# Performance work log

Measured on AMD Instinct MI355X. Metric: run time of the kernel, lower is better.

The kernel has to match this reference:

```python
import jax, jax.numpy as jnp
import numpy as np

B, BEAM, TMAX, V, D, H, NL, S, DFF = 4, 5, 16, 50257, 768, 12, 2, 128, 3072
BUF = TMAX + 1  # prefix buffer: sos + TMAX generated tokens
DH = D // H
SOS, EOS = 1, 2
NEG = -1e20


def _ln(x, g, b):
    m = x.mean(-1, keepdims=True)
    v = ((x - m) ** 2).mean(-1, keepdims=True)
    return (x - m) / jnp.sqrt(v + 1e-5) * g + b


def _mha(q_in, kv_in, in_w, in_b, out_w, out_b, bias=None, kpm=None):
    # PyTorch-style MHA: packed in_proj [3D, D], out_proj [D, D]
    q = q_in @ in_w[:D].T + in_b[:D]
    k = kv_in @ in_w[D:2 * D].T + in_b[D:2 * D]
    v = kv_in @ in_w[2 * D:].T + in_b[2 * D:]
    Bq, Tq = q.shape[0], q.shape[1]
    Tk = k.shape[1]
    q = q.reshape(Bq, Tq, H, DH)
    k = k.reshape(Bq, Tk, H, DH)
    v = v.reshape(Bq, Tk, H, DH)
    s = jnp.einsum('bqhd,bkhd->bhqk', q, k) * (1.0 / np.sqrt(DH))
    if bias is not None:
        s = s + bias  # additive causal bias (-10000 * (1 - tril)), as in source
    if kpm is not None:
        s = jnp.where(kpm[:, None, None, :], -1e9, s)  # memory_key_padding_mask
    a = jax.nn.softmax(s, axis=-1)
    o = jnp.einsum('bhqk,bkhd->bqhd', a, v).reshape(Bq, Tq, D)
    return o @ out_w.T + out_b


def _decode(emb, pos, ln_emb_g, ln_emb_b, self_in_w, self_in_b, self_out_w,
            self_out_b, cross_in_w, cross_in_b, cross_out_w, cross_out_b,
            ff1_w, ff1_b, ff2_w, ff2_b, ln1_g, ln1_b, ln2_g, ln2_b, ln3_g,
            ln3_b, dense_w, dense_b, context, source_mask):
    causal = -10000.0 * (1.0 - jnp.tril(jnp.ones((BUF, BUF), jnp.float32)))
    mem = jnp.repeat(context, BEAM, axis=0)            # [B*BEAM, S, D]
    kpm = jnp.repeat(source_mask == 0, BEAM, axis=0)   # True = pad
    # Beam init: nextYs[0] = [sos, 0, 0, ...]; scores trick makes step-0 pick
    # from beam row 0 only, matching beamLk = wordLk[0] in the source.
    buf0 = jnp.zeros((B, BEAM, BUF), jnp.int32).at[:, 0, 0].set(SOS)
    s0 = jnp.concatenate([jnp.zeros((1,), jnp.float32),
                          jnp.full((BEAM - 1,), NEG, jnp.float32)])
    scores0 = jnp.broadcast_to(s0, (B, BEAM))

    def step(carry, t):
        scores, buf = carry
        # no KV cache: re-run full decoder each step (fixed-size padded buffer;
        # causal mask makes positions <= t identical to running on the prefix)
        x = emb[buf.reshape(B * BEAM, BUF)] + pos[None, :BUF]
        x = _ln(x, ln_emb_g, ln_emb_b)
        for l in range(NL):  # post-norm TransformerDecoderLayer, dropout=eval
            sa = _mha(x, x, self_in_w[l], self_in_b[l], self_out_w[l],
                      self_out_b[l], bias=causal)
            x = _ln(x + sa, ln1_g[l], ln1_b[l])
            ca = _mha(x, mem, cross_in_w[l], cross_in_b[l], cross_out_w[l],
                      cross_out_b[l], kpm=kpm)
            x = _ln(x + ca, ln2_g[l], ln2_b[l])
            ff = jax.nn.relu(x @ ff1_w[l].T + ff1_b[l]) @ ff2_w[l].T + ff2_b[l]
            x = _ln(x + ff, ln3_g[l], ln3_b[l])
        h = jnp.tanh(jnp.take(x, t, axis=1) @ dense_w.T + dense_b)  # last pos
        logp = jax.nn.log_softmax(h @ emb.T, axis=-1).reshape(B, BEAM, V)
        last = jnp.take(buf, t, axis=2)  # previous token per beam
        beamLk = logp + scores[:, :, None]
        beamLk = jnp.where((last == EOS)[:, :, None], NEG, beamLk)
        vals, ids = jax.lax.top_k(beamLk.reshape(B, BEAM * V), BEAM)
        prevK = ids // V
        tok = (ids % V).astype(jnp.int32)
        buf = jnp.take_along_axis(buf, prevK[:, :, None], axis=1)
        buf = buf.at[:, :, t + 1].set(tok)
        return (vals, buf), None

    (scores, buf), _ = jax.lax.scan(step, (scores0, buf0), jnp.arange(TMAX))
    toks = buf[:, :, 1:]                         # backtracked hypotheses
    keep = jnp.cumsum(toks == EOS, axis=-1) == 0  # truncate at eos, pad with 0
    preds = jnp.where(keep, toks, 0)
    return scores, preds


def setup_inputs() -> dict:
    key = jax.random.key(0)
    ks = jax.random.split(key, 12)
    r = lambda k, shape: jax.random.normal(k, shape, jnp.float32) * 0.02
    inp = {}
    inp['emb'] = r(ks[0], (V, D))
    inp['pos'] = r(ks[1], (BUF, D))
    inp['ln_emb_g'] = jnp.ones((D,), jnp.float32)
    inp['ln_emb_b'] = jnp.zeros((D,), jnp.float32)
    inp['self_in_w'] = r(ks[2], (NL, 3 * D, D))
    inp['self_in_b'] = jnp.zeros((NL, 3 * D), jnp.float32)
    inp['self_out_w'] = r(ks[3], (NL, D, D))
    inp['self_out_b'] = jnp.zeros((NL, D), jnp.float32)
    inp['cross_in_w'] = r(ks[4], (NL, 3 * D, D))
    inp['cross_in_b'] = jnp.zeros((NL, 3 * D), jnp.float32)
    inp['cross_out_w'] = r(ks[5], (NL, D, D))
    inp['cross_out_b'] = jnp.zeros((NL, D), jnp.float32)
    inp['ff1_w'] = r(ks[6], (NL, DFF, D))
    inp['ff1_b'] = jnp.zeros((NL, DFF), jnp.float32)
    inp['ff2_w'] = r(ks[7], (NL, D, DFF))
    inp['ff2_b'] = jnp.zeros((NL, D), jnp.float32)
    inp['ln1_g'] = jnp.ones((NL, D), jnp.float32)
    inp['ln1_b'] = jnp.zeros((NL, D), jnp.float32)
    inp['ln2_g'] = jnp.ones((NL, D), jnp.float32)
    inp['ln2_b'] = jnp.zeros((NL, D), jnp.float32)
    inp['ln3_g'] = jnp.ones((NL, D), jnp.float32)
    inp['ln3_b'] = jnp.zeros((NL, D), jnp.float32)
    inp['dense_w'] = r(ks[8], (D, D))
    inp['dense_b'] = jnp.zeros((D,), jnp.float32)
    inp['context'] = jax.random.normal(ks[9], (B, S, D), jnp.float32)
    inp['source_mask'] = jnp.ones((B, S), jnp.int32)
    return inp


def reference(emb, pos, ln_emb_g, ln_emb_b, self_in_w, self_in_b, self_out_w,
              self_out_b, cross_in_w, cross_in_b, cross_out_w, cross_out_b,
              ff1_w, ff1_b, ff2_w, ff2_b, ln1_g, ln1_b, ln2_g, ln2_b, ln3_g,
              ln3_b, dense_w, dense_b, context, source_mask):
    return _decode(emb, pos, ln_emb_g, ln_emb_b, self_in_w, self_in_b,
                   self_out_w, self_out_b, cross_in_w, cross_in_b,
                   cross_out_w, cross_out_b, ff1_w, ff1_b, ff2_w, ff2_b,
                   ln1_g, ln1_b, ln2_g, ln2_b, ln3_g, ln3_b, dense_w,
                   dense_b, context, source_mask)
```

## Files before the change

### kernel.cpp

```cpp
#include <hip/hip_runtime.h>
#include <cfloat>
#include <cmath>

constexpr int kV   = 50257;
constexpr int kVP  = 50432;
constexpr int kD   = 768;
constexpr int NLY  = 2;
constexpr int BB   = 4;
constexpr int BEAM = 5;
constexpr int RR   = BB * BEAM;
constexpr int BUFL = 17;
constexpr int SS   = 128;
constexpr int DFF  = 3072;
constexpr int TMAX = 16;
constexpr int SOS  = 1;
constexpr int EOSt = 2;
constexpr int LB   = (kV + 255) / 256;
#define NEGV (-1e20f)

__device__ inline float wave_sum(float v) {
#pragma unroll
  for (int o = 32; o > 0; o >>= 1) v += __shfl_xor(v, o, 64);
  return v;
}
__device__ inline float wave_max(float v) {
#pragma unroll
  for (int o = 32; o > 0; o >>= 1) v = fmaxf(v, __shfl_xor(v, o, 64));
  return v;
}
__device__ inline bool better(float v1, int i1, float v2, int i2) {
  return v1 > v2 || (v1 == v2 && i1 < i2);
}
__device__ inline void insert5(float* tv, int* ti, float v, int i) {
  if (better(v, i, tv[4], ti[4])) {
    tv[4] = v; ti[4] = i;
#pragma unroll
    for (int s = 4; s > 0; --s)
      if (better(tv[s], ti[s], tv[s - 1], ti[s - 1])) {
        float fv = tv[s]; tv[s] = tv[s - 1]; tv[s - 1] = fv;
        int iv = ti[s]; ti[s] = ti[s - 1]; ti[s - 1] = iv;
      }
  }
}
__device__ inline float sel5f(const float* a, int i) {
  float r = a[0];
  r = (i == 1) ? a[1] : r; r = (i == 2) ? a[2] : r;
  r = (i == 3) ? a[3] : r; r = (i == 4) ? a[4] : r;
  return r;
}
__device__ inline int sel5i(const int* a, int i) {
  int r = a[0];
  r = (i == 1) ? a[1] : r; r = (i == 2) ? a[2] : r;
  r = (i == 3) ? a[3] : r; r = (i == 4) ? a[4] : r;
  return r;
}
__device__ inline void merge5(float* av, int* ai, const float* bv, const int* bi) {
  float cv[5]; int ci[5];
  int ia = 0, ib = 0;
#pragma unroll
  for (int s = 0; s < 5; ++s) {
    float va = sel5f(av, ia); int xa = sel5i(ai, ia);
    float vb = sel5f(bv, ib); int xb = sel5i(bi, ib);
    bool ta = better(va, xa, vb, xb);
    cv[s] = ta ? va : vb; ci[s] = ta ? xa : xb;
    ia += ta ? 1 : 0; ib += ta ? 0 : 1;
  }
#pragma unroll
  for (int s = 0; s < 5; ++s) { av[s] = cv[s]; ai[s] = ci[s]; }
}

__global__ void init_k(int* buf0, float* scores) {
  int tid = threadIdx.x;
  if (tid < RR * BUFL) buf0[tid] = 0;
  __syncthreads();
  if (tid < BB) buf0[tid * BEAM * BUFL] = SOS;
  if (tid < RR) scores[tid] = (tid % BEAM == 0) ? 0.f : NEGV;
}

__global__ void transpose_k(const float* __restrict__ src, float* __restrict__ dst,
                            int R, int C, int ds) {
  __shared__ float tile[32][33];
  const int c0 = blockIdx.x * 32, r0 = blockIdx.y * 32;
  const int lx = threadIdx.x & 31, ly = threadIdx.x >> 5;
#pragma unroll
  for (int j = 0; j < 4; ++j) {
    int r = r0 + ly + j * 8;
    if (r < R && c0 + lx < C) tile[ly + j * 8][lx] = src[(size_t)r * C + c0 + lx];
  }
  __syncthreads();
#pragma unroll
  for (int j = 0; j < 4; ++j) {
    int c = c0 + ly + j * 8;
    if (c < C && r0 + lx < R) dst[(size_t)c * ds + r0 + lx] = tile[lx][ly + j * 8];
  }
}

template<bool WT>
__global__ __launch_bounds__(256) void crosskv_k(
    const float* __restrict__ ctx, const float* __restrict__ Wm0,
    const float* __restrict__ bias0, float* __restrict__ ck, float* __restrict__ cv) {
  const int l = blockIdx.z;
  const float* Wm = Wm0 + (size_t)l * 2304 * 768;
  const float* bias = bias0 + l * 2304;
  __shared__ float a_s[16 * 768];
  __shared__ float ps[4 * 64 * 17];
  const int tid = threadIdx.x;
  const int row0 = blockIdx.y * 16;
  for (int i = tid * 4; i < 16 * 768; i += 1024) {
    int rr = i / 768, k = i - rr * 768;
    *(float4*)&a_s[i] = *(const float4*)&ctx[(size_t)(row0 + rr) * 768 + k];
  }
  __syncthreads();
  const int w = tid >> 6, lane = tid & 63;
  const int colg = 768 + blockIdx.x * 64 + lane;
  const int kb = w * 192;
  float acc[16];
#pragma unroll
  for (int r = 0; r < 16; ++r) acc[r] = 0.f;
  for (int k4 = 0; k4 < 48; ++k4) {
    const int k = kb + k4 * 4;
    float w0, w1, w2, w3;
    if (WT) {
      w0 = Wm[(size_t)(k + 0) * 2304 + colg]; w1 = Wm[(size_t)(k + 1) * 2304 + colg];
      w2 = Wm[(size_t)(k + 2) * 2304 + colg]; w3 = Wm[(size_t)(k + 3) * 2304 + colg];
    } else {
      float4 wv = *(const float4*)&Wm[(size_t)colg * 768 + k];
      w0 = wv.x; w1 = wv.y; w2 = wv.z; w3 = wv.w;
    }
#pragma unroll
    for (int r = 0; r < 16; ++r) {
      float4 a = *(const float4*)&a_s[r * 768 + k];
      acc[r] = fmaf(a.x, w0, fmaf(a.y, w1, fmaf(a.z, w2, fmaf(a.w, w3, acc[r]))));
    }
  }
#pragma unroll
  for (int r = 0; r < 16; ++r) ps[(w * 64 + lane) * 17 + r] = acc[r];
  __syncthreads();
  for (int o = tid; o < 1024; o += 256) {
    int rr = o >> 6, cl = o & 63;
    int cg = 768 + blockIdx.x * 64 + cl;
    float v = bias[cg];
#pragma unroll
    for (int ww = 0; ww < 4; ++ww) v += ps[(ww * 64 + cl) * 17 + rr];
    int gr = row0 + rr;
    int b = gr >> 7, s = gr & 127;
    int c = cg - 768, kv = c / 768, n = c - kv * 768;
    float* dst = kv ? cv : ck;
    dst[((size_t)(l * 4 + b) * 128 + s) * 768 + n] = v;
  }
}

template<bool WT>
__global__ __launch_bounds__(256) void gemm20_k(
    const float* __restrict__ Wm, int wstride, const float* __restrict__ bias, int N,
    int pre, const float* __restrict__ xsrc, const float* __restrict__ tmp_in,
    const float* __restrict__ lng, const float* __restrict__ lnb, float* __restrict__ xout,
    int outmode, float* __restrict__ out0,
    float* __restrict__ kcl, float* __restrict__ vcl, int t,
    const float* __restrict__ embp, const float* __restrict__ posw, const int* __restrict__ bufn,
    int reorder_t, const float* __restrict__ kco, const float* __restrict__ vco,
    float* __restrict__ kcn, float* __restrict__ vcn, const int* __restrict__ prevK) {
  __shared__ float a_s[RR * 768];
  __shared__ float ps[4 * 64 * 21];
  __shared__ float mS[RR], rS[RR];
  __shared__ int tokS[RR];
  const int tid = threadIdx.x;

  if (reorder_t > 0) {
    const int per = 768 * reorder_t;
    const int tot = 2 * RR * per;
    for (int i = blockIdx.x * 256 + tid; i < tot; i += gridDim.x * 256) {
      int half = i / (RR * per);
      int rem = i - half * RR * per;
      int r = rem / per;
      int rem2 = rem - r * per;
      int p = rem2 / 768;
      int d = rem2 - p * 768;
      int src = (r / BEAM) * BEAM + prevK[r];
      if (half == 0) kcn[(r * BUFL + p) * 768 + d] = kco[(src * BUFL + p) * 768 + d];
      else           vcn[(r * BUFL + p) * 768 + d] = vco[(src * BUFL + p) * 768 + d];
    }
  }
  if (pre == 1 && tid < RR) tokS[tid] = bufn[tid * BUFL + t];
  __syncthreads();
  for (int i = tid * 4; i < RR * 768; i += 1024) {
    int r = i / 768, k = i - r * 768;
    float4 v;
    if (pre == 0) v = *(const float4*)&xsrc[i];
    else if (pre == 1) {
      float4 e = *(const float4*)&embp[(size_t)tokS[r] * 768 + k];
      float4 p = *(const float4*)&posw[(size_t)t * 768 + k];
      v = make_float4(e.x + p.x, e.y + p.y, e.z + p.z, e.w + p.w);
    } else {
      float4 a = *(const float4*)&xsrc[i];
      float4 b = *(const float4*)&tmp_in[i];
      v = make_float4(a.x + b.x, a.y + b.y, a.z + b.z, a.w + b.w);
    }
    *(float4*)&a_s[i] = v;
  }
  __syncthreads();
  if (pre != 0) {
    const int w0 = tid >> 6, ln = tid & 63;
    for (int r = w0 * 5; r < w0 * 5 + 5; ++r) {
      float s = 0.f, q = 0.f;
      for (int k = ln; k < 768; k += 64) { float v = a_s[r * 768 + k]; s += v; q += v * v; }
      s = wave_sum(s); q = wave_sum(q);
      if (ln == 0) {
        float m = s / 768.f;
        float var = q / 768.f - m * m;
        mS[r] = m; rS[r] = 1.f / sqrtf(var + 1e-5f);
      }
    }
    __syncthreads();
    for (int i = tid * 4; i < RR * 768; i += 1024) {
      int r = i / 768, k = i - r * 768;
      float4 v = *(const float4*)&a_s[i];
      float4 g = *(const float4*)&lng[k];
      float4 b = *(const float4*)&lnb[k];
      float m = mS[r], rs = rS[r];
      v = make_float4((v.x - m) * rs * g.x + b.x, (v.y - m) * rs * g.y + b.y,
                      (v.z - m) * rs * g.z + b.z, (v.w - m) * rs * g.w + b.w);
      *(float4*)&a_s[i] = v;
    }
    __syncthreads();
    if (xout != nullptr && blockIdx.x == 0) {
      for (int i = tid * 4; i < RR * 768; i += 1024)
        *(float4*)&xout[i] = *(const float4*)&a_s[i];
    }
  }
  const int w = tid >> 6, lane = tid & 63;
  const int colg = blockIdx.x * 64 + lane;
  const int kb = w * 192;
  float acc[RR];
#pragma unroll
  for (int r = 0; r < RR; ++r) acc[r] = 0.f;
  for (int k4 = 0; k4 < 48; ++k4) {
    const int k = kb + k4 * 4;
    float w0, w1, w2, w3;
    if (WT) {
      w0 = Wm[(size_t)(k + 0) * wstride + colg]; w1 = Wm[(size_t)(k + 1) * wstride + colg];
      w2 = Wm[(size_t)(k + 2) * wstride + colg]; w3 = Wm[(size_t)(k + 3) * wstride + colg];
    } else {
      float4 wv = *(const float4*)&Wm[(size_t)colg * 768 + k];
      w0 = wv.x; w1 = wv.y; w2 = wv.z; w3 = wv.w;
    }
#pragma unroll
    for (int r = 0; r < RR; ++r) {
      float4 a = *(const float4*)&a_s[r * 768 + k];
      acc[r] = fmaf(a.x, w0, fmaf(a.y, w1, fmaf(a.z, w2, fmaf(a.w, w3, acc[r]))));
    }
  }
#pragma unroll
  for (int r = 0; r < RR; ++r) ps[(w * 64 + lane) * 21 + r] = acc[r];
  __syncthreads();
  for (int o = tid; o < RR * 64; o += 256) {
    int r = o >> 6, cl = o & 63;
    int cg = blockIdx.x * 64 + cl;
    float v = bias[cg];
#pragma unroll
    for (int ww = 0; ww < 4; ++ww) v += ps[(ww * 64 + cl) * 21 + r];
    if (outmode == 1) v = fmaxf(v, 0.f);
    else if (outmode == 2) v = tanhf(v);
    if (outmode == 3) {
      if (cg < 768) out0[r * 768 + cg];
      if (cg < 768) out0[r * 768 + cg] = v;
      else if (cg < 1536) kcl[(r * BUFL + t) * 768 + (cg - 768)] = v;
      else vcl[(r * BUFL + t) * 768 + (cg - 1536)] = v;
    } else {
      out0[(size_t)r * N + cg] = v;
    }
  }
}

template<bool WT>
__global__ __launch_bounds__(1024) void ff2_k(
    const float* __restrict__ Wm, const float* __restrict__ bias,
    const float* __restrict__ A, float* __restrict__ out0) {
  __shared__ float ps[64 * 16 * 21];
  const int tid = threadIdx.x;
  const int w = tid >> 6, lane = tid & 63;
  const int cl = lane & 15, ksub = lane >> 4;
  const int colg = blockIdx.x * 16 + cl;
  const int kb = w * 192 + ksub * 48;
  float acc[RR];
#pragma unroll
  for (int r = 0; r < RR; ++r) acc[r] = 0.f;
  for (int k4 = 0; k4 < 12; ++k4) {
    const int k = kb + k4 * 4;
    float w0, w1, w2, w3;
    if (WT) {
      w0 = Wm[(size_t)(k + 0) * 768 + colg]; w1 = Wm[(size_t)(k + 1) * 768 + colg];
      w2 = Wm[(size_t)(k + 2) * 768 + colg]; w3 = Wm[(size_t)(k + 3) * 768 + colg];
    } else {
      float4 wv = *(const float4*)&Wm[(size_t)colg * 3072 + k];
      w0 = wv.x; w1 = wv.y; w2 = wv.z; w3 = wv.w;
    }
#pragma unroll
    for (int r = 0; r < RR; ++r) {
      float4 a = *(const float4*)&A[r * 3072 + k];
      acc[r] = fmaf(a.x, w0, fmaf(a.y, w1, fmaf(a.z, w2, fmaf(a.w, w3, acc[r]))));
    }
  }
  const int seg = w * 4 + ksub;
#pragma unroll
  for (int r = 0; r < RR; ++r) ps[(seg * 16 + cl) * 21 + r] = acc[r];
  __syncthreads();
  if (tid < RR * 16) {
    int r = tid >> 4, c2 = tid & 15;
    float v = bias[blockIdx.x * 16 + c2];
    for (int s2 = 0; s2 < 64; ++s2) v += ps[(s2 * 16 + c2) * 21 + r];
    out0[r * 768 + blockIdx.x * 16 + c2] = v;
  }
}

__global__ __launch_bounds__(64) void self_attn_k(
    const float* __restrict__ qb, const float* __restrict__ kcn,
    const float* __restrict__ vcn, float* __restrict__ outb, int t) {
  const int r = blockIdx.x, hh = blockIdx.y, lane = threadIdx.x;
  __shared__ float qs[64];
  __shared__ float ks[16 * 65];
  __shared__ float pp[16];
  qs[lane] = qb[r * 768 + hh * 64 + lane];
  for (int p = 0; p <= t; ++p)
    ks[p * 65 + lane] = kcn[(r * BUFL + p) * 768 + hh * 64 + lane];
  __syncthreads();
  float s = -1e30f;
  if (lane <= t) {
    float a = 0.f;
#pragma unroll
    for (int d = 0; d < 64; ++d) a = fmaf(qs[d], ks[lane * 65 + d], a);
    s = a * 0.125f;
  }
  float m = wave_max(s);
  float p = expf(s - m);
  float sum = wave_sum(p);
  if (lane <= t) pp[lane] = p / sum;
  __syncthreads();
  const float* vb = vcn + r * BUFL * 768 + hh * 64 + lane;
  float o = 0.f;
  for (int k = 0; k <= t; ++k) o = fmaf(pp[k], vb[k * 768], o);
  outb[r * 768 + hh * 64 + lane] = o;
}

__global__ __launch_bounds__(64) void cross_attn_k(
    const float* __restrict__ qb, const float* __restrict__ ck,
    const float* __restrict__ cv, const int* __restrict__ smask,
    float* __restrict__ outb) {
  const int r = blockIdx.x, hh = blockIdx.y, lane = threadIdx.x;
  const int b = r / BEAM;
  __shared__ float qs[64];
  __shared__ float ks[128 * 65];
  __shared__ float pp[128];
  qs[lane] = qb[r * 768 + hh * 64 + lane];
  for (int p = 0; p < 128; ++p)
    ks[p * 65 + lane] = ck[((size_t)b * 128 + p) * 768 + hh * 64 + lane];
  __syncthreads();
  float a0 = 0.f, a1 = 0.f;
#pragma unroll
  for (int d = 0; d < 64; ++d) {
    a0 = fmaf(qs[d], ks[lane * 65 + d], a0);
    a1 = fmaf(qs[d], ks[(lane + 64) * 65 + d], a1);
  }
  float s0 = a0 * 0.125f, s1 = a1 * 0.125f;
  if (smask[b * 128 + lane] == 0)      s0 = -1e9f;
  if (smask[b * 128 + lane + 64] == 0) s1 = -1e9f;
  float m = wave_max(fmaxf(s0, s1));
  float p0 = expf(s0 - m), p1 = expf(s1 - m);
  float sum = wave_sum(p0 + p1);
  pp[lane] = p0 / sum; pp[lane + 64] = p1 / sum;
  __syncthreads();
  const float* vb = cv + (size_t)b * 128 * 768 + hh * 64 + lane;
  float o0 = 0.f, o1 = 0.f, o2 = 0.f, o3 = 0.f;
  for (int k = 0; k < 128; k += 4) {
    o0 = fmaf(pp[k + 0], vb[(k + 0) * 768], o0);
    o1 = fmaf(pp[k + 1], vb[(k + 1) * 768], o1);
    o2 = fmaf(pp[k + 2], vb[(k + 2) * 768], o2);
    o3 = fmaf(pp[k + 3], vb[(k + 3) * 768], o3);
  }
  outb[r * 768 + hh * 64 + lane] = (o0 + o1) + (o2 + o3);
}

template<bool ET>
__global__ __launch_bounds__(256) void logits_k(
    const float* __restrict__ hbuf, const float* __restrict__ embM,
    float* __restrict__ candV, int* __restrict__ candI,
    float* __restrict__ mrow, float* __restrict__ srow) {
  __shared__ float hs[RR * 768];
  __shared__ float vv[4 * 256];
  const int tid = threadIdx.x, blk = blockIdx.x;
  for (int i = tid * 4; i < RR * 768; i += 1024)
    *(float4*)&hs[i] = *(const float4*)&hbuf[i];
  __syncthreads();
  const int col = blk * 256 + tid;
  const bool valid = col < kV;
  const int colc = valid ? col : (kV - 1);
  float acc[RR];
#pragma unroll
  for (int r = 0; r < RR; ++r) acc[r] = 0.f;
  for (int k = 0; k < 768; k += 4) {
    float w0, w1, w2, w3;
    if (ET) {
      w0 = embM[(size_t)(k + 0) * kVP + col]; w1 = embM[(size_t)(k + 1) * kVP + col];
      w2 = embM[(size_t)(k + 2) * kVP + col]; w3 = embM[(size_t)(k + 3) * kVP + col];
    } else {
      float4 wv = *(const float4*)&embM[(size_t)colc * 768 + k];
      w0 = wv.x; w1 = wv.y; w2 = wv.z; w3 = wv.w;
    }
#pragma unroll
    for (int r = 0; r < RR; ++r) {
      float4 a = *(const float4*)&hs[r * 768 + k];
      acc[r] = fmaf(a.x, w0, fmaf(a.y, w1, fmaf(a.z, w2, fmaf(a.w, w3, acc[r]))));
    }
  }
  const int w = tid >> 6, lane = tid & 63;
  for (int g = 0; g < 5; ++g) {
#pragma unroll
    for (int j = 0; j < 4; ++j) vv[j * 256 + tid] = valid ? acc[g * 4 + j] : -FLT_MAX;
    __syncthreads();
    const int r = g * 4 + w;
    float v[4]; int gc[4]; bool used[4];
#pragma unroll
    for (int j = 0; j < 4; ++j) {
      v[j] = vv[w * 256 + lane * 4 + j];
      gc[j] = blk * 256 + lane * 4 + j;
      used[j] = false;
    }
    float tv[5]; int tg[5];
#pragma unroll
    for (int round = 0; round < 5; ++round) {
      float bv = -FLT_MAX; int bidx = 0x7fffffff; int bj = -1;
#pragma unroll
      for (int j = 0; j < 4; ++j) {
        bool c = (!used[j]) && better(v[j], gc[j], bv, bidx);
        bv = c ? v[j] : bv; bidx = c ? gc[j] : bidx; bj = c ? j : bj;
      }
      float wv2 = bv; int wi = bidx;
      for (int d = 1; d < 64; d <<= 1) {
        float ov = __shfl_xor(wv2, d, 64); int oi = __shfl_xor(wi, d, 64);
        if (better(ov, oi, wv2, wi)) { wv2 = ov; wi = oi; }
      }
      tv[round] = wv2; tg[round] = wi;
      if (bj >= 0 && bidx == wi) used[bj] = true;
    }
    float m = tv[0];
    float s = 0.f;
#pragma unroll
    for (int j = 0; j < 4; ++j) s += expf(v[j] - m);
    s = wave_sum(s);
    if (lane == 0) {
      mrow[r * LB + blk] = m;
      srow[r * LB + blk] = s;
#pragma unroll
      for (int q = 0; q < 5; ++q) {
        candV[(r * LB + blk) * 5 + q] = tv[q];
        candI[(r * LB + blk) * 5 + q] = tg[q];
      }
    }
    __syncthreads();
  }
}

__global__ __launch_bounds__(256) void topk_k(
    const float* __restrict__ candV, const int* __restrict__ candI,
    const float* __restrict__ mrow, const float* __restrict__ srow,
    float* __restrict__ scores, const int* __restrict__ bufc, int* __restrict__ bufn,
    int t, int* __restrict__ prevK, int* __restrict__ tokv) {
  const int b = blockIdx.x, tid = threadIdx.x;
  const int w = tid >> 6, lane = tid & 63;
  __shared__ float lseS[5], scS[5];
  __shared__ int emS[5];
  __shared__ float wv5[4][5]; __shared__ int wi5[4][5];
  __shared__ int fpk[5], ftok[5];
  for (int j = w; j < 5; j += 4) {
    const int gr = b * 5 + j;
    float M = -FLT_MAX, S = 0.f;
    for (int e = lane; e < LB; e += 64) {
      float m2 = mrow[gr * LB + e], s2 = srow[gr * LB + e];
      if (m2 > M) { S = S * expf(M - m2) + s2; M = m2; }
      else        { S += s2 * expf(m2 - M); }
    }
    for (int d = 1; d < 64; d <<= 1) {
      float Mo = __shfl_xor(M, d, 64), So = __shfl_xor(S, d, 64);
      float Mn = fmaxf(M, Mo);
      S = S * expf(M - Mn) + So * expf(Mo - Mn);
      M = Mn;
    }
    if (lane == 0) {
      lseS[j] = M + logf(S);
      scS[j] = scores[gr];
      emS[j] = (bufc[gr * BUFL + t] == EOSt);
    }
  }
  __syncthreads();
  float tv[5]; int ti[5];
#pragma unroll
  for (int s = 0; s < 5; ++s) { tv[s] = -FLT_MAX; ti[s] = 0x7fffffff; }
  for (int i = tid; i < 5 * LB * 5; i += 256) {
    int j = i / (LB * 5);
    int e = i - j * LB * 5;
    int blk = e / 5, rk = e - blk * 5;
    int gr = b * 5 + j;
    float cvv = candV[(gr * LB + blk) * 5 + rk];
    int col = candI[(gr * LB + blk) * 5 + rk];
    float val = emS[j] ? NEGV : (cvv - lseS[j] + scS[j]);
    insert5(tv, ti, val, j * kV + col);
  }
  for (int d = 1; d < 64; d <<= 1) {
    float ov[5]; int oi[5];
#pragma unroll
    for (int s = 0; s < 5; ++s) { ov[s] = __shfl_xor(tv[s], d, 64); oi[s] = __shfl_xor(ti[s], d, 64); }
    merge5(tv, ti, ov, oi);
  }
  if (lane == 0) {
#pragma unroll
    for (int s = 0; s < 5; ++s) { wv5[w][s] = tv[s]; wi5[w][s] = ti[s]; }
  }
  __syncthreads();
  if (tid == 0) {
    float av[5]; int ai[5];
#pragma unroll
    for (int s = 0; s < 5; ++s) { av[s] = wv5[0][s]; ai[s] = wi5[0][s]; }
    for (int ww = 1; ww < 4; ++ww) {
      float bv[5]; int bi[5];
#pragma unroll
      for (int s = 0; s < 5; ++s) { bv[s] = wv5[ww][s]; bi[s] = wi5[ww][s]; }
      merge5(av, ai, bv, bi);
    }
#pragma unroll
    for (int s = 0; s < 5; ++s) {
      int pk = ai[s] / kV;
      int tk = ai[s] - pk * kV;
      scores[b * 5 + s] = av[s];
      prevK[b * 5 + s] = pk; tokv[b * 5 + s] = tk;
      fpk[s] = pk; ftok[s] = tk;
    }
  }
  __syncthreads();
  for (int i = tid; i < 5 * BUFL; i += 256) {
    int j = i / BUFL, p = i - j * BUFL;
    int src = b * 5 + fpk[j];
    int val = (p == t + 1) ? ftok[j] : bufc[src * BUFL + p];
    bufn[(b * 5 + j) * BUFL + p] = val;
  }
}

__global__ void finalize_k(const float* __restrict__ scores, const int* __restrict__ buf,
                           float* __restrict__ out) {
  const int tid = threadIdx.x;
  if (tid < RR) {
    out[tid] = scores[tid];
    int seen = 0;
    for (int i = 0; i < TMAX; ++i) {
      int tk = buf[tid * BUFL + 1 + i];
      if (tk == EOSt) seen = 1;
      out[RR + tid * TMAX + i] = seen ? 0.f : (float)tk;
    }
  }
}

extern "C" void kernel_launch(void* const* d_in, const int* in_sizes, int n_in,
                              void* d_out, int out_size, void* d_ws, size_t ws_size,
                              hipStream_t stream) {
  const float* emb        = (const float*)d_in[0];
  const float* pos        = (const float*)d_in[1];
  const float* ln_emb_g   = (const float*)d_in[2];
  const float* ln_emb_b   = (const float*)d_in[3];
  const float* self_in_w  = (const float*)d_in[4];
  const float* self_in_b  = (const float*)d_in[5];
  const float* self_out_w = (const float*)d_in[6];
  const float* self_out_b = (const float*)d_in[7];
  const float* cross_in_w = (const float*)d_in[8];
  const float* cross_in_b = (const float*)d_in[9];
  const float* cross_out_w= (const float*)d_in[10];
  const float* cross_out_b= (const float*)d_in[11];
  const float* ff1_w      = (const float*)d_in[12];
  const float* ff1_b      = (const float*)d_in[13];
  const float* ff2_w      = (const float*)d_in[14];
  const float* ff2_b      = (const float*)d_in[15];
  const float* ln1_g      = (const float*)d_in[16];
  const float* ln1_b      = (const float*)d_in[17];
  const float* ln2_g      = (const float*)d_in[18];
  const float* ln2_b      = (const float*)d_in[19];
  const float* ln3_g      = (const float*)d_in[20];
  const float* ln3_b      = (const float*)d_in[21];
  const float* dense_w    = (const float*)d_in[22];
  const float* dense_b    = (const float*)d_in[23];
  const float* context    = (const float*)d_in[24];
  const int*   source_mask= (const int*)d_in[25];

  float* wsf = (float*)d_ws;
  size_t off = 0;
  auto alloc = [&](size_t n) { float* p = wsf + off; off += (n + 3) & ~(size_t)3; return p; };

  float* XA    = alloc(RR * 768);
  float* XB    = alloc(RR * 768);
  float* XC    = alloc(RR * 768);
  float* qb    = alloc(RR * 768);
  float* attnb = alloc(RR * 768);
  float* tmp   = alloc(RR * 768);
  float* hbuf  = alloc(RR * 768);
  float* ffb   = alloc(RR * 3072);
  float* candV = alloc(RR * LB * 5);
  float* mrow  = alloc(RR * LB);
  float* srow  = alloc(RR * LB);
  float* scores= alloc(32);
  float* ck    = alloc((size_t)NLY * 4 * 128 * 768);
  float* cv    = alloc((size_t)NLY * 4 * 128 * 768);
  const size_t cacheSeg = (size_t)RR * BUFL * 768;
  float* kcB   = alloc(4 * cacheSeg);
  float* vcB   = alloc(4 * cacheSeg);
  int* candI   = (int*)alloc(RR * LB * 5);
  int* bufs0   = (int*)alloc(RR * BUFL + 12);
  int* bufs1   = (int*)alloc(RR * BUFL + 12);
  int* prevKp  = (int*)alloc(32);
  int* tokp    = (int*)alloc(32);
  const size_t baseFloats = off;

  const size_t nSiT = (size_t)768 * 2304, nSoT = (size_t)768 * 768;
  const size_t nCiT = nSiT, nCoT = nSoT, nF1T = (size_t)768 * 3072, nF2T = (size_t)3072 * 768;
  const size_t wtFloats = 2 * (nSiT + nSoT + nCiT + nCoT + nF1T + nF2T) + nSoT;
  const size_t embTFloats = (size_t)768 * kVP;
  const bool useWT = ws_size >= (baseFloats + wtFloats) * 4;
  const bool useET = useWT && ws_size >= (baseFloats + wtFloats + embTFloats) * 4;

  float* siT[2]; float* soT[2]; float* ciT[2]; float* coT[2]; float* f1T[2]; float* f2T[2];
  float* dT = nullptr; float* embT = nullptr;
  if (useWT) {
    for (int l = 0; l < 2; ++l) siT[l] = alloc(nSiT);
    for (int l = 0; l < 2; ++l) soT[l] = alloc(nSoT);
    for (int l = 0; l < 2; ++l) ciT[l] = alloc(nCiT);
    for (int l = 0; l < 2; ++l) coT[l] = alloc(nCoT);
    for (int l = 0; l < 2; ++l) f1T[l] = alloc(nF1T);
    for (int l = 0; l < 2; ++l) f2T[l] = alloc(nF2T);
    dT = alloc(nSoT);
    if (useET) embT = alloc(embTFloats);
  }

  init_k<<<1, 512, 0, stream>>>(bufs0, scores);

  if (useWT) {
    auto T = [&](const float* src, float* dst, int R, int C, int ds) {
      dim3 g((C + 31) / 32, (R + 31) / 32);
      transpose_k<<<g, 256, 0, stream>>>(src, dst, R, C, ds);
    };
    for (int l = 0; l < 2; ++l) {
      T(self_in_w  + (size_t)l * 2304 * 768, siT[l], 2304, 768, 2304);
      T(self_out_w + (size_t)l * 768 * 768,  soT[l], 768, 768, 768);
      T(cross_in_w + (size_t)l * 2304 * 768, ciT[l], 2304, 768, 2304);
      T(cross_out_w+ (size_t)l * 768 * 768,  coT[l], 768, 768, 768);
      T(ff1_w      + (size_t)l * 3072 * 768, f1T[l], 3072, 768, 3072);
      T(ff2_w      + (size_t)l * 768 * 3072, f2T[l], 768, 3072, 768);
    }
    T(dense_w, dT, 768, 768, 768);
    if (useET) T(emb, embT, kV, 768, kVP);
  }

  {
    dim3 g(24, 32, 2);
    if (useWT) crosskv_k<true><<<g, 256, 0, stream>>>(context, ciT[0], cross_in_b, ck, cv);
    else       crosskv_k<false><<<g, 256, 0, stream>>>(context, cross_in_w, cross_in_b, ck, cv);
  }

  const int* bc = bufs0;
  auto G = [&](const float* Wt, const float* Wg, int wstride,
               const float* bias, int N, int pre, const float* xsrc, const float* tmpin,
               const float* g2, const float* b2, float* xout, int outmode, float* out0,
               float* kcl, float* vcl, int tt,
               int reorder_t, const float* kco, const float* vco, float* kcn2, float* vcn2) {
    dim3 grid(N / 64);
    if (useWT)
      gemm20_k<true><<<grid, 256, 0, stream>>>(Wt, wstride, bias, N, pre, xsrc, tmpin, g2, b2,
        xout, outmode, out0, kcl, vcl, tt, emb, pos, bc, reorder_t, kco, vco, kcn2, vcn2, prevKp);
    else
      gemm20_k<false><<<grid, 256, 0, stream>>>(Wg, wstride, bias, N, pre, xsrc, tmpin, g2, b2,
        xout, outmode, out0, kcl, vcl, tt, emb, pos, bc, reorder_t, kco, vco, kcn2, vcn2, prevKp);
  };

  for (int t = 0; t < TMAX; ++t) {
    bc = (t & 1) ? bufs1 : bufs0;
    int* bn = (t & 1) ? bufs0 : bufs1;
    const int np = (t + 1) & 1, op = t & 1;

    for (int l = 0; l < 2; ++l) {
      float* kNew = kcB + (np * 2 + l) * cacheSeg;
      float* vNew = vcB + (np * 2 + l) * cacheSeg;
      float* kOld = kcB + (op * 2 + l) * cacheSeg;
      float* vOld = vcB + (op * 2 + l) * cacheSeg;
      if (l == 0)
        G(siT[0], self_in_w, 2304, self_in_b, 2304,
          1, nullptr, nullptr, ln_emb_g, ln_emb_b, XA,
          3, qb, kNew, vNew, t, t, kOld, vOld, kNew, vNew);
      else
        G(siT[1], self_in_w + (size_t)2304 * 768, 2304, self_in_b + 2304, 2304,
          2, XC, tmp, ln3_g, ln3_b, XA,
          3, qb, kNew, vNew, t, t, kOld, vOld, kNew, vNew);
      self_attn_k<<<dim3(RR, 12), 64, 0, stream>>>(qb, kNew, vNew, attnb, t);
      G(soT[l], self_out_w + (size_t)l * 768 * 768, 768, self_out_b + l * 768, 768,
        0, attnb, nullptr, nullptr, nullptr, nullptr, 0, tmp,
        nullptr, nullptr, t, 0, nullptr, nullptr, nullptr, nullptr);
      G(ciT[l], cross_in_w + (size_t)l * 2304 * 768, 2304, cross_in_b + l * 2304, 768,
        2, XA, tmp, ln1_g + l * 768, ln1_b + l * 768, XB, 0, qb,
        nullptr, nullptr, t, 0, nullptr, nullptr, nullptr, nullptr);
      cross_attn_k<<<dim3(RR, 12), 64, 0, stream>>>(
          qb, ck + (size_t)l * 4 * 128 * 768, cv + (size_t)l * 4 * 128 * 768, source_mask, attnb);
      G(coT[l], cross_out_w + (size_t)l * 768 * 768, 768, cross_out_b + l * 768, 768,
        0, attnb, nullptr, nullptr, nullptr, nullptr, 0, tmp,
        nullptr, nullptr, t, 0, nullptr, nullptr, nullptr, nullptr);
      G(f1T[l], ff1_w + (size_t)l * 3072 * 768, 3072, ff1_b + l * 3072, 3072,
        2, XB, tmp, ln2_g + l * 768, ln2_b + l * 768, XC, 1, ffb,
        nullptr, nullptr, t, 0, nullptr, nullptr, nullptr, nullptr);
      if (useWT) ff2_k<true><<<48, 1024, 0, stream>>>(f2T[l], ff2_b + l * 768, ffb, tmp);
      else       ff2_k<false><<<48, 1024, 0, stream>>>(ff2_w + (size_t)l * 768 * 3072, ff2_b + l * 768, ffb, tmp);
    }
    G(dT, dense_w, 768, dense_b, 768,
      2, XC, tmp, ln3_g + 768, ln3_b + 768, nullptr, 2, hbuf,
      nullptr, nullptr, t, 0, nullptr, nullptr, nullptr, nullptr);
    if (useET) logits_k<true><<<LB, 256, 0, stream>>>(hbuf, embT, candV, candI, mrow, srow);
    else       logits_k<false><<<LB, 256, 0, stream>>>(hbuf, emb, candV, candI, mrow, srow);
    topk_k<<<BB, 256, 0, stream>>>(candV, candI, mrow, srow, scores, bc, bn, t, prevKp, tokp);
  }

  finalize_k<<<1, 64, 0, stream>>>(scores, bufs0, (float*)d_out);
}
```

Before: 11.20 ms.

## Fuse whole beam-search decode into a persistent megakernel with grid barriers

```diff
diff --git a/kernel.cpp b/kernel.cpp
--- a/kernel.cpp
+++ b/kernel.cpp
@@ -4,34 +4,31 @@
 
 constexpr int kV   = 50257;
 constexpr int kVP  = 50432;
-constexpr int kD   = 768;
-constexpr int NLY  = 2;
 constexpr int BB   = 4;
 constexpr int BEAM = 5;
-constexpr int RR   = BB * BEAM;
+constexpr int RR   = 20;
 constexpr int BUFL = 17;
-constexpr int SS   = 128;
-constexpr int DFF  = 3072;
 constexpr int TMAX = 16;
 constexpr int SOS  = 1;
 constexpr int EOSt = 2;
 constexpr int LB   = (kV + 255) / 256;
+constexpr int CSEG = RR * BUFL * 768;
 #define NEGV (-1e20f)
 
-__device__ inline float wave_sum(float v) {
+__device__ __forceinline__ float wave_sum(float v) {
 #pragma unroll
   for (int o = 32; o > 0; o >>= 1) v += __shfl_xor(v, o, 64);
   return v;
 }
-__device__ inline float wave_max(float v) {
+__device__ __forceinline__ float wave_max(float v) {
 #pragma unroll
   for (int o = 32; o > 0; o >>= 1) v = fmaxf(v, __shfl_xor(v, o, 64));
   return v;
 }
-__device__ inline bool better(float v1, int i1, float v2, int i2) {
+__device__ __forceinline__ bool better(float v1, int i1, float v2, int i2) {
   return v1 > v2 || (v1 == v2 && i1 < i2);
 }
-__device__ inline void insert5(float* tv, int* ti, float v, int i) {
+__device__ __forceinline__ void insert5(float* tv, int* ti, float v, int i) {
   if (better(v, i, tv[4], ti[4])) {
     tv[4] = v; ti[4] = i;
 #pragma unroll
@@ -42,19 +39,19 @@
       }
   }
 }
-__device__ inline float sel5f(const float* a, int i) {
+__device__ __forceinline__ float sel5f(const float* a, int i) {
   float r = a[0];
   r = (i == 1) ? a[1] : r; r = (i == 2) ? a[2] : r;
   r = (i == 3) ? a[3] : r; r = (i == 4) ? a[4] : r;
   return r;
 }
-__device__ inline int sel5i(const int* a, int i) {
+__device__ __forceinline__ int sel5i(const int* a, int i) {
   int r = a[0];
   r = (i == 1) ? a[1] : r; r = (i == 2) ? a[2] : r;
   r = (i == 3) ? a[3] : r; r = (i == 4) ? a[4] : r;
   return r;
 }
-__device__ inline void merge5(float* av, int* ai, const float* bv, const int* bi) {
+__device__ __forceinline__ void merge5(float* av, int* ai, const float* bv, const int* bi) {
   float cv[5]; int ci[5];
   int ia = 0, ib = 0;
 #pragma unroll
@@ -69,327 +66,340 @@
   for (int s = 0; s < 5; ++s) { av[s] = cv[s]; ai[s] = ci[s]; }
 }
 
-__global__ void init_k(int* buf0, float* scores) {
-  int tid = threadIdx.x;
-  if (tid < RR * BUFL) buf0[tid] = 0;
-  __syncthreads();
-  if (tid < BB) buf0[tid * BEAM * BUFL] = SOS;
-  if (tid < RR) scores[tid] = (tid % BEAM == 0) ? 0.f : NEGV;
-}
-
-__global__ void transpose_k(const float* __restrict__ src, float* __restrict__ dst,
-                            int R, int C, int ds) {
-  __shared__ float tile[32][33];
-  const int c0 = blockIdx.x * 32, r0 = blockIdx.y * 32;
-  const int lx = threadIdx.x & 31, ly = threadIdx.x >> 5;
-#pragma unroll
-  for (int j = 0; j < 4; ++j) {
-    int r = r0 + ly + j * 8;
-    if (r < R && c0 + lx < C) tile[ly + j * 8][lx] = src[(size_t)r * C + c0 + lx];
-  }
-  __syncthreads();
-#pragma unroll
-  for (int j = 0; j < 4; ++j) {
-    int c = c0 + ly + j * 8;
-    if (c < C && r0 + lx < R) dst[(size_t)c * ds + r0 + lx] = tile[lx][ly + j * 8];
+struct KParams {
+  const float *emb, *pos, *lneg, *lneb;
+  const float *siW, *siB, *soW, *soB, *ciW, *ciB, *coW, *coB;
+  const float *f1W, *f1B, *f2W, *f2B;
+  const float *ln1g, *ln1b, *ln2g, *ln2b, *ln3g, *ln3b;
+  const float *dW, *dB, *ctx;
+  const int* smask;
+  float *XA, *XB, *XC, *qb, *attnb, *tmp, *hbuf, *ffb;
+  float *fp0, *fp1, *fp2, *fp3;
+  float *candV, *mrow, *srow, *scores, *ck, *cv, *kcB, *vcB;
+  int *candI, *bufs0, *bufs1, *prevK, *tokv;
+  int *arrive, *release;
+  float *out;
+  float *siT, *soT, *ciT, *coT, *f1T, *f2T, *dT, *embT;
+  int useWT, useET;
+};
+
+__device__ __forceinline__ void gbar(int* arr, int* rel, int& ph) {
+  ++ph;
+  __syncthreads();
+  if (threadIdx.x == 0) {
+    __threadfence();
+    __hip_atomic_store(&arr[blockIdx.x], ph, __ATOMIC_RELAXED, __HIP_MEMORY_SCOPE_AGENT);
+  }
+  if (blockIdx.x == 0) {
+    while (__hip_atomic_load(&arr[threadIdx.x], __ATOMIC_RELAXED, __HIP_MEMORY_SCOPE_AGENT) < ph)
+      __builtin_amdgcn_s_sleep(2);
+    __syncthreads();
+    if (threadIdx.x == 0) {
+      __threadfence();
+      __hip_atomic_store(rel, ph, __ATOMIC_RELAXED, __HIP_MEMORY_SCOPE_AGENT);
+    }
+    __syncthreads();
+  } else {
+    if (threadIdx.x == 0) {
+      while (__hip_atomic_load(rel, __ATOMIC_RELAXED, __HIP_MEMORY_SCOPE_AGENT) < ph)
+        __builtin_amdgcn_s_sleep(2);
+      __threadfence();
+    }
+    __syncthreads();
+  }
+}
+
+__device__ void do_transposes(const KParams& P, float* SM) {
+  const float* srcs[14]; float* dsts[14]; int Rs[14], Cs[14], dss[14];
+  int nj = 0;
+  for (int l = 0; l < 2; ++l) { srcs[nj]=P.siW + (size_t)l*2304*768; dsts[nj]=P.siT + (size_t)l*768*2304; Rs[nj]=2304; Cs[nj]=768; dss[nj]=2304; ++nj; }
+  for (int l = 0; l < 2; ++l) { srcs[nj]=P.soW + (size_t)l*768*768;  dsts[nj]=P.soT + (size_t)l*768*768;  Rs[nj]=768;  Cs[nj]=768; dss[nj]=768;  ++nj; }
+  for (int l = 0; l < 2; ++l) { srcs[nj]=P.ciW + (size_t)l*2304*768; dsts[nj]=P.ciT + (size_t)l*768*2304; Rs[nj]=2304; Cs[nj]=768; dss[nj]=2304; ++nj; }
+  for (int l = 0; l < 2; ++l) { srcs[nj]=P.coW + (size_t)l*768*768;  dsts[nj]=P.coT + (size_t)l*768*768;  Rs[nj]=768;  Cs[nj]=768; dss[nj]=768;  ++nj; }
+  for (int l = 0; l < 2; ++l) { srcs[nj]=P.f1W + (size_t)l*3072*768; dsts[nj]=P.f1T + (size_t)l*768*3072; Rs[nj]=3072; Cs[nj]=768; dss[nj]=3072; ++nj; }
+  for (int l = 0; l < 2; ++l) { srcs[nj]=P.f2W + (size_t)l*768*3072; dsts[nj]=P.f2T + (size_t)l*3072*768; Rs[nj]=768;  Cs[nj]=3072; dss[nj]=768; ++nj; }
+  srcs[nj]=P.dW; dsts[nj]=P.dT; Rs[nj]=768; Cs[nj]=768; dss[nj]=768; ++nj;
+  if (P.useET) { srcs[nj]=P.emb; dsts[nj]=P.embT; Rs[nj]=kV; Cs[nj]=768; dss[nj]=kVP; ++nj; }
+  int tcnt[14], tot = 0;
+  for (int j = 0; j < nj; ++j) { tcnt[j] = ((Rs[j]+31)/32) * ((Cs[j]+31)/32); tot += tcnt[j]; }
+  const int tid = threadIdx.x;
+  const int lx = tid & 31, ly = tid >> 5;
+  for (int jt = blockIdx.x; jt < tot; jt += 256) {
+    int j = 0, lt = jt;
+    while (lt >= tcnt[j]) { lt -= tcnt[j]; ++j; }
+    int ct = (Cs[j] + 31) / 32;
+    int tr = lt / ct, tc = lt - tr * ct;
+    const float* src = srcs[j]; float* dst = dsts[j];
+    int R = Rs[j], C = Cs[j], ds = dss[j];
+    int r0 = tr * 32, c0 = tc * 32;
+    __syncthreads();
+#pragma unroll
+    for (int q = 0; q < 4; ++q) {
+      int r = r0 + ly + q * 8;
+      if (r < R && c0 + lx < C) SM[(ly + q * 8) * 33 + lx] = src[(size_t)r * C + c0 + lx];
+    }
+    __syncthreads();
+#pragma unroll
+    for (int q = 0; q < 4; ++q) {
+      int c = c0 + ly + q * 8;
+      if (c < C && r0 + lx < R) dst[(size_t)c * ds + r0 + lx] = SM[lx * 33 + ly + q * 8];
+    }
   }
 }
 
 template<bool WT>
-__global__ __launch_bounds__(256) void crosskv_k(
-    const float* __restrict__ ctx, const float* __restrict__ Wm0,
-    const float* __restrict__ bias0, float* __restrict__ ck, float* __restrict__ cv) {
-  const int l = blockIdx.z;
-  const float* Wm = Wm0 + (size_t)l * 2304 * 768;
-  const float* bias = bias0 + l * 2304;
-  __shared__ float a_s[16 * 768];
-  __shared__ float ps[4 * 64 * 17];
-  const int tid = threadIdx.x;
-  const int row0 = blockIdx.y * 16;
-  for (int i = tid * 4; i < 16 * 768; i += 1024) {
-    int rr = i / 768, k = i - rr * 768;
-    *(float4*)&a_s[i] = *(const float4*)&ctx[(size_t)(row0 + rr) * 768 + k];
-  }
-  __syncthreads();
-  const int w = tid >> 6, lane = tid & 63;
-  const int colg = 768 + blockIdx.x * 64 + lane;
-  const int kb = w * 192;
-  float acc[16];
-#pragma unroll
-  for (int r = 0; r < 16; ++r) acc[r] = 0.f;
-  for (int k4 = 0; k4 < 48; ++k4) {
-    const int k = kb + k4 * 4;
-    float w0, w1, w2, w3;
-    if (WT) {
-      w0 = Wm[(size_t)(k + 0) * 2304 + colg]; w1 = Wm[(size_t)(k + 1) * 2304 + colg];
-      w2 = Wm[(size_t)(k + 2) * 2304 + colg]; w3 = Wm[(size_t)(k + 3) * 2304 + colg];
-    } else {
-      float4 wv = *(const float4*)&Wm[(size_t)colg * 768 + k];
-      w0 = wv.x; w1 = wv.y; w2 = wv.z; w3 = wv.w;
-    }
-#pragma unroll
-    for (int r = 0; r < 16; ++r) {
-      float4 a = *(const float4*)&a_s[r * 768 + k];
-      acc[r] = fmaf(a.x, w0, fmaf(a.y, w1, fmaf(a.z, w2, fmaf(a.w, w3, acc[r]))));
-    }
-  }
-#pragma unroll
-  for (int r = 0; r < 16; ++r) ps[(w * 64 + lane) * 17 + r] = acc[r];
-  __syncthreads();
-  for (int o = tid; o < 1024; o += 256) {
-    int rr = o >> 6, cl = o & 63;
-    int cg = 768 + blockIdx.x * 64 + cl;
-    float v = bias[cg];
-#pragma unroll
-    for (int ww = 0; ww < 4; ++ww) v += ps[(ww * 64 + cl) * 17 + rr];
-    int gr = row0 + rr;
-    int b = gr >> 7, s = gr & 127;
-    int c = cg - 768, kv = c / 768, n = c - kv * 768;
-    float* dst = kv ? cv : ck;
-    dst[((size_t)(l * 4 + b) * 128 + s) * 768 + n] = v;
-  }
-}
-
-template<bool WT>
-__global__ __launch_bounds__(256) void gemm20_k(
-    const float* __restrict__ Wm, int wstride, const float* __restrict__ bias, int N,
-    int pre, const float* __restrict__ xsrc, const float* __restrict__ tmp_in,
-    const float* __restrict__ lng, const float* __restrict__ lnb, float* __restrict__ xout,
-    int outmode, float* __restrict__ out0,
-    float* __restrict__ kcl, float* __restrict__ vcl, int t,
-    const float* __restrict__ embp, const float* __restrict__ posw, const int* __restrict__ bufn,
-    int reorder_t, const float* __restrict__ kco, const float* __restrict__ vco,
-    float* __restrict__ kcn, float* __restrict__ vcn, const int* __restrict__ prevK) {
-  __shared__ float a_s[RR * 768];
-  __shared__ float ps[4 * 64 * 21];
-  __shared__ float mS[RR], rS[RR];
-  __shared__ int tokS[RR];
-  const int tid = threadIdx.x;
-
-  if (reorder_t > 0) {
-    const int per = 768 * reorder_t;
-    const int tot = 2 * RR * per;
-    for (int i = blockIdx.x * 256 + tid; i < tot; i += gridDim.x * 256) {
-      int half = i / (RR * per);
-      int rem = i - half * RR * per;
-      int r = rem / per;
-      int rem2 = rem - r * per;
-      int p = rem2 / 768;
-      int d = rem2 - p * 768;
-      int src = (r / BEAM) * BEAM + prevK[r];
-      if (half == 0) kcn[(r * BUFL + p) * 768 + d] = kco[(src * BUFL + p) * 768 + d];
-      else           vcn[(r * BUFL + p) * 768 + d] = vco[(src * BUFL + p) * 768 + d];
-    }
-  }
-  if (pre == 1 && tid < RR) tokS[tid] = bufn[tid * BUFL + t];
-  __syncthreads();
-  for (int i = tid * 4; i < RR * 768; i += 1024) {
-    int r = i / 768, k = i - r * 768;
-    float4 v;
-    if (pre == 0) v = *(const float4*)&xsrc[i];
-    else if (pre == 1) {
-      float4 e = *(const float4*)&embp[(size_t)tokS[r] * 768 + k];
-      float4 p = *(const float4*)&posw[(size_t)t * 768 + k];
-      v = make_float4(e.x + p.x, e.y + p.y, e.z + p.z, e.w + p.w);
-    } else {
-      float4 a = *(const float4*)&xsrc[i];
-      float4 b = *(const float4*)&tmp_in[i];
-      v = make_float4(a.x + b.x, a.y + b.y, a.z + b.z, a.w + b.w);
-    }
-    *(float4*)&a_s[i] = v;
-  }
-  __syncthreads();
-  if (pre != 0) {
-    const int w0 = tid >> 6, ln = tid & 63;
-    for (int r = w0 * 5; r < w0 * 5 + 5; ++r) {
-      float s = 0.f, q = 0.f;
-      for (int k = ln; k < 768; k += 64) { float v = a_s[r * 768 + k]; s += v; q += v * v; }
-      s = wave_sum(s); q = wave_sum(q);
-      if (ln == 0) {
-        float m = s / 768.f;
-        float var = q / 768.f - m * m;
-        mS[r] = m; rS[r] = 1.f / sqrtf(var + 1e-5f);
-      }
-    }
-    __syncthreads();
-    for (int i = tid * 4; i < RR * 768; i += 1024) {
-      int r = i / 768, k = i - r * 768;
-      float4 v = *(const float4*)&a_s[i];
-      float4 g = *(const float4*)&lng[k];
-      float4 b = *(const float4*)&lnb[k];
-      float m = mS[r], rs = rS[r];
-      v = make_float4((v.x - m) * rs * g.x + b.x, (v.y - m) * rs * g.y + b.y,
-                      (v.z - m) * rs * g.z + b.z, (v.w - m) * rs * g.w + b.w);
-      *(float4*)&a_s[i] = v;
-    }
-    __syncthreads();
-    if (xout != nullptr && blockIdx.x == 0) {
-      for (int i = tid * 4; i < RR * 768; i += 1024)
-        *(float4*)&xout[i] = *(const float4*)&a_s[i];
-    }
-  }
-  const int w = tid >> 6, lane = tid & 63;
-  const int colg = blockIdx.x * 64 + lane;
-  const int kb = w * 192;
-  float acc[RR];
-#pragma unroll
-  for (int r = 0; r < RR; ++r) acc[r] = 0.f;
-  for (int k4 = 0; k4 < 48; ++k4) {
-    const int k = kb + k4 * 4;
-    float w0, w1, w2, w3;
-    if (WT) {
-      w0 = Wm[(size_t)(k + 0) * wstride + colg]; w1 = Wm[(size_t)(k + 1) * wstride + colg];
-      w2 = Wm[(size_t)(k + 2) * wstride + colg]; w3 = Wm[(size_t)(k + 3) * wstride + colg];
-    } else {
-      float4 wv = *(const float4*)&Wm[(size_t)colg * 768 + k];
-      w0 = wv.x; w1 = wv.y; w2 = wv.z; w3 = wv.w;
-    }
-#pragma unroll
-    for (int r = 0; r < RR; ++r) {
-      float4 a = *(const float4*)&a_s[r * 768 + k];
-      acc[r] = fmaf(a.x, w0, fmaf(a.y, w1, fmaf(a.z, w2, fmaf(a.w, w3, acc[r]))));
-    }
-  }
-#pragma unroll
-  for (int r = 0; r < RR; ++r) ps[(w * 64 + lane) * 21 + r] = acc[r];
-  __syncthreads();
-  for (int o = tid; o < RR * 64; o += 256) {
-    int r = o >> 6, cl = o & 63;
-    int cg = blockIdx.x * 64 + cl;
-    float v = bias[cg];
-#pragma unroll
-    for (int ww = 0; ww < 4; ++ww) v += ps[(ww * 64 + cl) * 21 + r];
-    if (outmode == 1) v = fmaxf(v, 0.f);
-    else if (outmode == 2) v = tanhf(v);
-    if (outmode == 3) {
-      if (cg < 768) out0[r * 768 + cg];
-      if (cg < 768) out0[r * 768 + cg] = v;
-      else if (cg < 1536) kcl[(r * BUFL + t) * 768 + (cg - 768)] = v;
-      else vcl[(r * BUFL + t) * 768 + (cg - 1536)] = v;
-    } else {
-      out0[(size_t)r * N + cg] = v;
-    }
-  }
-}
-
-template<bool WT>
-__global__ __launch_bounds__(1024) void ff2_k(
-    const float* __restrict__ Wm, const float* __restrict__ bias,
-    const float* __restrict__ A, float* __restrict__ out0) {
-  __shared__ float ps[64 * 16 * 21];
+__device__ void do_crosskv(const KParams& P, float* SM) {
+  float* a_s = SM;
+  float* ps  = SM + 12288;
   const int tid = threadIdx.x;
   const int w = tid >> 6, lane = tid & 63;
-  const int cl = lane & 15, ksub = lane >> 4;
-  const int colg = blockIdx.x * 16 + cl;
-  const int kb = w * 192 + ksub * 48;
-  float acc[RR];
-#pragma unroll
-  for (int r = 0; r < RR; ++r) acc[r] = 0.f;
-  for (int k4 = 0; k4 < 12; ++k4) {
-    const int k = kb + k4 * 4;
-    float w0, w1, w2, w3;
-    if (WT) {
-      w0 = Wm[(size_t)(k + 0) * 768 + colg]; w1 = Wm[(size_t)(k + 1) * 768 + colg];
-      w2 = Wm[(size_t)(k + 2) * 768 + colg]; w3 = Wm[(size_t)(k + 3) * 768 + colg];
-    } else {
-      float4 wv = *(const float4*)&Wm[(size_t)colg * 3072 + k];
-      w0 = wv.x; w1 = wv.y; w2 = wv.z; w3 = wv.w;
-    }
-#pragma unroll
-    for (int r = 0; r < RR; ++r) {
-      float4 a = *(const float4*)&A[r * 3072 + k];
-      acc[r] = fmaf(a.x, w0, fmaf(a.y, w1, fmaf(a.z, w2, fmaf(a.w, w3, acc[r]))));
-    }
-  }
-  const int seg = w * 4 + ksub;
-#pragma unroll
-  for (int r = 0; r < RR; ++r) ps[(seg * 16 + cl) * 21 + r] = acc[r];
-  __syncthreads();
-  if (tid < RR * 16) {
-    int r = tid >> 4, c2 = tid & 15;
-    float v = bias[blockIdx.x * 16 + c2];
-    for (int s2 = 0; s2 < 64; ++s2) v += ps[(s2 * 16 + c2) * 21 + r];
-    out0[r * 768 + blockIdx.x * 16 + c2] = v;
-  }
-}
-
-__global__ __launch_bounds__(64) void self_attn_k(
-    const float* __restrict__ qb, const float* __restrict__ kcn,
-    const float* __restrict__ vcn, float* __restrict__ outb, int t) {
-  const int r = blockIdx.x, hh = blockIdx.y, lane = threadIdx.x;
-  __shared__ float qs[64];
-  __shared__ float ks[16 * 65];
-  __shared__ float pp[16];
-  qs[lane] = qb[r * 768 + hh * 64 + lane];
-  for (int p = 0; p <= t; ++p)
-    ks[p * 65 + lane] = kcn[(r * BUFL + p) * 768 + hh * 64 + lane];
+  for (int i5 = 0; i5 < 6; ++i5) {
+    int j = blockIdx.x + 256 * i5;
+    int cx = j % 24, ry = (j / 24) % 32, l = j / 768;
+    const float* Wt = P.ciT + (size_t)l * 768 * 2304;
+    const float* Wg = P.ciW + (size_t)l * 2304 * 768;
+    const float* bias = P.ciB + l * 2304;
+    const int row0 = ry * 16;
+    __syncthreads();
+    for (int i = tid * 4; i < 16 * 768; i += 1024) {
+      int rr = i / 768, k = i - rr * 768;
+      *(float4*)&a_s[i] = *(const float4*)&P.ctx[(size_t)(row0 + rr) * 768 + k];
+    }
+    __syncthreads();
+    const int colg = 768 + cx * 64 + lane;
+    const int kb = w * 192;
+    float acc[16];
+#pragma unroll
+    for (int r = 0; r < 16; ++r) acc[r] = 0.f;
+    for (int k4 = 0; k4 < 48; ++k4) {
+      const int k = kb + k4 * 4;
+      float w0, w1, w2, w3;
+      if (WT) {
+        const float* wr = Wt + (size_t)k * 2304 + colg;
+        w0 = wr[0]; w1 = wr[2304]; w2 = wr[2 * 2304]; w3 = wr[3 * 2304];
+      } else {
+        float4 wv = *(const float4*)&Wg[(size_t)colg * 768 + k];
+        w0 = wv.x; w1 = wv.y; w2 = wv.z; w3 = wv.w;
+      }
+#pragma unroll
+      for (int r = 0; r < 16; ++r) {
+        float4 a = *(const float4*)&a_s[r * 768 + k];
+        acc[r] = fmaf(a.x, w0, fmaf(a.y, w1, fmaf(a.z, w2, fmaf(a.w, w3, acc[r]))));
+      }
+    }
+#pragma unroll
+    for (int r = 0; r < 16; ++r) ps[(w * 64 + lane) * 16 + r] = acc[r];
+    __syncthreads();
+    for (int o = tid; o < 1024; o += 256) {
+      int rr = o >> 6, cl = o & 63;
+      int cg = 768 + cx * 64 + cl;
+      float v = bias[cg];
+#pragma unroll
+      for (int ww = 0; ww < 4; ++ww) v += ps[(ww * 64 + cl) * 16 + rr];
+      int gr = row0 + rr;
+      int b = gr >> 7, s = gr & 127;
+      int c = cg - 768, kv = c / 768, n = c - kv * 768;
+      float* dst = kv ? P.cv : P.ck;
+      dst[((size_t)(l * 4 + b) * 128 + s) * 768 + n] = v;
+    }
+  }
+}
+
+template<bool WT>
+__device__ void gemm_tile(
+    float* SM, int tile,
+    const float* Wt, int wstride, const float* Wg, int wgK, int wRowOff,
+    const float* bias, bool addBias,
+    int pre, const float* aBase, int aStride,
+    const float* xsrc, const float* const* parts, int nparts,
+    const float* lng, const float* lnb, float* xout,
+    int outmode, float* out0, int Nout,
+    float* kNew, float* vNew, int t, const int* bufc,
+    const float* embw, const float* posw)
+{
+  float* a_s = SM;
+  float* ps  = SM + 7680;
+  float* mS  = SM + 12800;
+  float* rS  = SM + 12820;
+  int* tokS  = (int*)(SM + 12840);
+  const int tid = threadIdx.x;
+  const int w = tid >> 6, lane = tid & 63;
+  if (pre == 1 && tid < RR) tokS[tid] = bufc[tid * BUFL + t];
+  __syncthreads();
+  for (int rp = 0; rp < 2; ++rp) {
+    const int r0 = rp * 10;
+    for (int i = tid * 4; i < 7680; i += 1024) {
+      int rl = i / 768, k = i - rl * 768, r = r0 + rl;
+      float4 v;
+      if (pre == 0) v = *(const float4*)&aBase[(size_t)r * aStride + k];
+      else if (pre == 1) {
+        float4 e = *(const float4*)&embw[(size_t)tokS[r] * 768 + k];
+        float4 p = *(const float4*)&posw[(size_t)t * 768 + k];
+        v = make_float4(e.x + p.x, e.y + p.y, e.z + p.z, e.w + p.w);
+      } else {
+        v = *(const float4*)&xsrc[r * 768 + k];
+        for (int q = 0; q < nparts; ++q) {
+          float4 u = *(const float4*)&parts[q][r * 768 + k];
+          v.x += u.x; v.y += u.y; v.z += u.z; v.w += u.w;
+        }
+      }
+      *(float4*)&a_s[i] = v;
+    }
+    __syncthreads();
+    if (pre != 0) {
+      for (int rl = w; rl < 10; rl += 4) {
+        float s = 0.f, q = 0.f;
+        for (int k = lane; k < 768; k += 64) { float v = a_s[rl * 768 + k]; s += v; q += v * v; }
+        s = wave_sum(s); q = wave_sum(q);
+        if (lane == 0) {
+          float m = s / 768.f;
+          mS[rl] = m; rS[rl] = 1.f / sqrtf(q / 768.f - m * m + 1e-5f);
+        }
+      }
+      __syncthreads();
+      for (int i = tid * 4; i < 7680; i += 1024) {
+        int rl = i / 768, k = i - rl * 768;
+        float4 v = *(const float4*)&a_s[i];
+        float4 g = *(const float4*)&lng[k];
+        float4 b = *(const float4*)&lnb[k];
+        float m = mS[rl], rs = rS[rl];
+        v = make_float4((v.x - m) * rs * g.x + b.x, (v.y - m) * rs * g.y + b.y,
+                        (v.z - m) * rs * g.z + b.z, (v.w - m) * rs * g.w + b.w);
+        *(float4*)&a_s[i] = v;
+        if (xout != nullptr && tile == 0) *(float4*)&xout[(r0 + rl) * 768 + k] = v;
+      }
+      __syncthreads();
+    }
+    const int c0 = tile * 128 + lane;
+    const int kb = w * 192;
+    float acc0[10], acc1[10];
+#pragma unroll
+    for (int rl = 0; rl < 10; ++rl) { acc0[rl] = 0.f; acc1[rl] = 0.f; }
+    for (int k4 = 0; k4 < 48; ++k4) {
+      const int k = kb + k4 * 4, kg = wRowOff + k;
+      float wa0, wa1, wa2, wa3, wb0, wb1, wb2, wb3;
+      if (WT) {
+        const float* wr = Wt + (size_t)kg * wstride;
+        wa0 = wr[c0]; wb0 = wr[c0 + 64]; wr += wstride;
+        wa1 = wr[c0]; wb1 = wr[c0 + 64]; wr += wstride;
+        wa2 = wr[c0]; wb2 = wr[c0 + 64]; wr += wstride;
+        wa3 = wr[c0]; wb3 = wr[c0 + 64];
+      } else {
+        float4 A4 = *(const float4*)&Wg[(size_t)c0 * wgK + kg];
+        float4 B4 = *(const float4*)&Wg[(size_t)(c0 + 64) * wgK + kg];
+        wa0 = A4.x; wa1 = A4.y; wa2 = A4.z; wa3 = A4.w;
+        wb0 = B4.x; wb1 = B4.y; wb2 = B4.z; wb3 = B4.w;
+      }
+#pragma unroll
+      for (int rl = 0; rl < 10; ++rl) {
+        float4 a = *(const float4*)&a_s[rl * 768 + k];
+        acc0[rl] = fmaf(a.x, wa0, fmaf(a.y, wa1, fmaf(a.z, wa2, fmaf(a.w, wa3, acc0[rl]))));
+        acc1[rl] = fmaf(a.x, wb0, fmaf(a.y, wb1, fmaf(a.z, wb2, fmaf(a.w, wb3, acc1[rl]))));
+      }
+    }
+#pragma unroll
+    for (int rl = 0; rl < 10; ++rl) {
+      ps[(w * 128 + lane) * 10 + rl] = acc0[rl];
+      ps[(w * 128 + 64 + lane) * 10 + rl] = acc1[rl];
+    }
+    __syncthreads();
+    for (int o = tid; o < 1280; o += 256) {
+      int rl = o >> 7, cl = o & 127;
+      int r = r0 + rl, cg = tile * 128 + cl;
+      float v = addBias ? bias[cg] : 0.f;
+#pragma unroll
+      for (int ww = 0; ww < 4; ++ww) v += ps[(ww * 128 + cl) * 10 + rl];
+      if (outmode == 1) v = fmaxf(v, 0.f);
+      else if (outmode == 2) v = tanhf(v);
+      if (outmode == 3) {
+        if (cg < 768) out0[r * 768 + cg] = v;
+        else if (cg < 1536) kNew[(r * BUFL + t) * 768 + (cg - 768)] = v;
+        else vNew[(r * BUFL + t) * 768 + (cg - 1536)] = v;
+      } else {
+        out0[(size_t)r * Nout + cg] = v;
+      }
+    }
+    __syncthreads();
+  }
+}
+
+__device__ void self_attn_phase(const KParams& P, float* SM, const float* kc, const float* vc, int t) {
+  const int tid = threadIdx.x;
+  const int w = tid >> 6, lane = tid & 63;
+  const int idx = blockIdx.x * 4 + w;
+  const int r = idx / 12, hh = idx - (idx / 12) * 12;
+  float* qsw = SM + w * 64;
+  float* ppw = SM + 256 + w * 128;
+  qsw[lane] = P.qb[r * 768 + hh * 64 + lane];
   __syncthreads();
   float s = -1e30f;
   if (lane <= t) {
+    const float* kr = kc + (size_t)(r * BUFL + lane) * 768 + hh * 64;
     float a = 0.f;
 #pragma unroll
-    for (int d = 0; d < 64; ++d) a = fmaf(qs[d], ks[lane * 65 + d], a);
+    for (int d4 = 0; d4 < 16; ++d4) {
+      float4 kk = *(const float4*)&kr[d4 * 4];
+      float4 qq = *(const float4*)&qsw[d4 * 4];
+      a = fmaf(qq.x, kk.x, fmaf(qq.y, kk.y, fmaf(qq.z, kk.z, fmaf(qq.w, kk.w, a))));
+    }
     s = a * 0.125f;
   }
   float m = wave_max(s);
   float p = expf(s - m);
   float sum = wave_sum(p);
-  if (lane <= t) pp[lane] = p / sum;
-  __syncthreads();
-  const float* vb = vcn + r * BUFL * 768 + hh * 64 + lane;
+  ppw[lane] = p / sum;
+  __syncthreads();
+  const float* vb = vc + (size_t)r * BUFL * 768 + hh * 64 + lane;
   float o = 0.f;
-  for (int k = 0; k <= t; ++k) o = fmaf(pp[k], vb[k * 768], o);
-  outb[r * 768 + hh * 64 + lane] = o;
-}
-
-__global__ __launch_bounds__(64) void cross_attn_k(
-    const float* __restrict__ qb, const float* __restrict__ ck,
-    const float* __restrict__ cv, const int* __restrict__ smask,
-    float* __restrict__ outb) {
-  const int r = blockIdx.x, hh = blockIdx.y, lane = threadIdx.x;
+  for (int k = 0; k <= t; ++k) o = fmaf(ppw[k], vb[k * 768], o);
+  P.attnb[r * 768 + hh * 64 + lane] = o;
+}
+
+__device__ void cross_attn_phase(const KParams& P, float* SM, const float* ck, const float* cv) {
+  const int tid = threadIdx.x;
+  const int w = tid >> 6, lane = tid & 63;
+  const int idx = blockIdx.x * 4 + w;
+  const int r = idx / 12, hh = idx - (idx / 12) * 12;
   const int b = r / BEAM;
-  __shared__ float qs[64];
-  __shared__ float ks[128 * 65];
-  __shared__ float pp[128];
-  qs[lane] = qb[r * 768 + hh * 64 + lane];
-  for (int p = 0; p < 128; ++p)
-    ks[p * 65 + lane] = ck[((size_t)b * 128 + p) * 768 + hh * 64 + lane];
+  float* qsw = SM + w * 64;
+  float* ppw = SM + 256 + w * 128;
+  qsw[lane] = P.qb[r * 768 + hh * 64 + lane];
   __syncthreads();
   float a0 = 0.f, a1 = 0.f;
-#pragma unroll
-  for (int d = 0; d < 64; ++d) {
-    a0 = fmaf(qs[d], ks[lane * 65 + d], a0);
-    a1 = fmaf(qs[d], ks[(lane + 64) * 65 + d], a1);
+  const float* k0 = ck + (size_t)(b * 128 + lane) * 768 + hh * 64;
+  const float* k1 = k0 + (size_t)64 * 768;
+#pragma unroll
+  for (int d4 = 0; d4 < 16; ++d4) {
+    float4 qq = *(const float4*)&qsw[d4 * 4];
+    float4 kk = *(const float4*)&k0[d4 * 4];
+    float4 k2 = *(const float4*)&k1[d4 * 4];
+    a0 = fmaf(qq.x, kk.x, fmaf(qq.y, kk.y, fmaf(qq.z, kk.z, fmaf(qq.w, kk.w, a0))));
+    a1 = fmaf(qq.x, k2.x, fmaf(qq.y, k2.y, fmaf(qq.z, k2.z, fmaf(qq.w, k2.w, a1))));
   }
   float s0 = a0 * 0.125f, s1 = a1 * 0.125f;
-  if (smask[b * 128 + lane] == 0)      s0 = -1e9f;
-  if (smask[b * 128 + lane + 64] == 0) s1 = -1e9f;
+  if (P.smask[b * 128 + lane] == 0)      s0 = -1e9f;
+  if (P.smask[b * 128 + lane + 64] == 0) s1 = -1e9f;
   float m = wave_max(fmaxf(s0, s1));
   float p0 = expf(s0 - m), p1 = expf(s1 - m);
   float sum = wave_sum(p0 + p1);
-  pp[lane] = p0 / sum; pp[lane + 64] = p1 / sum;
+  ppw[lane] = p0 / sum; ppw[lane + 64] = p1 / sum;
   __syncthreads();
   const float* vb = cv + (size_t)b * 128 * 768 + hh * 64 + lane;
-  float o0 = 0.f, o1 = 0.f, o2 = 0.f, o3 = 0.f;
-  for (int k = 0; k < 128; k += 4) {
-    o0 = fmaf(pp[k + 0], vb[(k + 0) * 768], o0);
-    o1 = fmaf(pp[k + 1], vb[(k + 1) * 768], o1);
-    o2 = fmaf(pp[k + 2], vb[(k + 2) * 768], o2);
-    o3 = fmaf(pp[k + 3], vb[(k + 3) * 768], o3);
-  }
-  outb[r * 768 + hh * 64 + lane] = (o0 + o1) + (o2 + o3);
+  float o0 = 0.f, o1 = 0.f;
+  for (int k = 0; k < 128; k += 2) {
+    o0 = fmaf(ppw[k], vb[k * 768], o0);
+    o1 = fmaf(ppw[k + 1], vb[(k + 1) * 768], o1);
+  }
+  P.attnb[r * 768 + hh * 64 + lane] = o0 + o1;
 }
 
 template<bool ET>
-__global__ __launch_bounds__(256) void logits_k(
-    const float* __restrict__ hbuf, const float* __restrict__ embM,
-    float* __restrict__ candV, int* __restrict__ candI,
-    float* __restrict__ mrow, float* __restrict__ srow) {
-  __shared__ float hs[RR * 768];
-  __shared__ float vv[4 * 256];
+__device__ void logits_phase(const KParams& P, float* SM) {
+  float* hs = SM;
+  float* vv = SM + 15360;
   const int tid = threadIdx.x, blk = blockIdx.x;
   for (int i = tid * 4; i < RR * 768; i += 1024)
-    *(float4*)&hs[i] = *(const float4*)&hbuf[i];
+    *(float4*)&hs[i] = *(const float4*)&P.hbuf[i];
   __syncthreads();
   const int col = blk * 256 + tid;
   const bool valid = col < kV;
@@ -400,10 +410,10 @@
   for (int k = 0; k < 768; k += 4) {
     float w0, w1, w2, w3;
     if (ET) {
-      w0 = embM[(size_t)(k + 0) * kVP + col]; w1 = embM[(size_t)(k + 1) * kVP + col];
-      w2 = embM[(size_t)(k + 2) * kVP + col]; w3 = embM[(size_t)(k + 3) * kVP + col];
+      w0 = P.embT[(size_t)(k + 0) * kVP + col]; w1 = P.embT[(size_t)(k + 1) * kVP + col];
+      w2 = P.embT[(size_t)(k + 2) * kVP + col]; w3 = P.embT[(size_t)(k + 3) * kVP + col];
     } else {
-      float4 wv = *(const float4*)&embM[(size_t)colc * 768 + k];
+      float4 wv = *(const float4*)&P.emb[(size_t)colc * 768 + k];
       w0 = wv.x; w1 = wv.y; w2 = wv.z; w3 = wv.w;
     }
 #pragma unroll
@@ -448,34 +458,33 @@
     for (int j = 0; j < 4; ++j) s += expf(v[j] - m);
     s = wave_sum(s);
     if (lane == 0) {
-      mrow[r * LB + blk] = m;
-      srow[r * LB + blk] = s;
+      P.mrow[r * LB + blk] = m;
+      P.srow[r * LB + blk] = s;
 #pragma unroll
       for (int q = 0; q < 5; ++q) {
-        candV[(r * LB + blk) * 5 + q] = tv[q];
-        candI[(r * LB + blk) * 5 + q] = tg[q];
-      }
-    }
-    __syncthreads();
-  }
-}
-
-__global__ __launch_bounds__(256) void topk_k(
-    const float* __restrict__ candV, const int* __restrict__ candI,
-    const float* __restrict__ mrow, const float* __restrict__ srow,
-    float* __restrict__ scores, const int* __restrict__ bufc, int* __restrict__ bufn,
-    int t, int* __restrict__ prevK, int* __restrict__ tokv) {
+        P.candV[(r * LB + blk) * 5 + q] = tv[q];
+        P.candI[(r * LB + blk) * 5 + q] = tg[q];
+      }
+    }
+    __syncthreads();
+  }
+}
+
+__device__ void topk_phase(const KParams& P, float* SM, const int* bufc, int* bufn, int t) {
   const int b = blockIdx.x, tid = threadIdx.x;
   const int w = tid >> 6, lane = tid & 63;
-  __shared__ float lseS[5], scS[5];
-  __shared__ int emS[5];
-  __shared__ float wv5[4][5]; __shared__ int wi5[4][5];
-  __shared__ int fpk[5], ftok[5];
+  float* lseS = SM;
+  float* scS  = SM + 8;
+  int*   emS  = (int*)(SM + 16);
+  float* wv5  = SM + 24;
+  int*   wi5  = (int*)(SM + 44);
+  int*   fpk  = (int*)(SM + 64);
+  int*   ftok = (int*)(SM + 72);
   for (int j = w; j < 5; j += 4) {
     const int gr = b * 5 + j;
     float M = -FLT_MAX, S = 0.f;
     for (int e = lane; e < LB; e += 64) {
-      float m2 = mrow[gr * LB + e], s2 = srow[gr * LB + e];
+      float m2 = P.mrow[gr * LB + e], s2 = P.srow[gr * LB + e];
       if (m2 > M) { S = S * expf(M - m2) + s2; M = m2; }
       else        { S += s2 * expf(m2 - M); }
     }
@@ -487,7 +496,7 @@
     }
     if (lane == 0) {
       lseS[j] = M + logf(S);
-      scS[j] = scores[gr];
+      scS[j] = P.scores[gr];
       emS[j] = (bufc[gr * BUFL + t] == EOSt);
     }
   }
@@ -497,11 +506,11 @@
   for (int s = 0; s < 5; ++s) { tv[s] = -FLT_MAX; ti[s] = 0x7fffffff; }
   for (int i = tid; i < 5 * LB * 5; i += 256) {
     int j = i / (LB * 5);
-    int e = i - j * LB * 5;
+    int e = i - j * (LB * 5);
     int blk = e / 5, rk = e - blk * 5;
     int gr = b * 5 + j;
-    float cvv = candV[(gr * LB + blk) * 5 + rk];
-    int col = candI[(gr * LB + blk) * 5 + rk];
+    float cvv = P.candV[(gr * LB + blk) * 5 + rk];
+    int col = P.candI[(gr * LB + blk) * 5 + rk];
     float val = emS[j] ? NEGV : (cvv - lseS[j] + scS[j]);
     insert5(tv, ti, val, j * kV + col);
   }
@@ -513,25 +522,25 @@
   }
   if (lane == 0) {
 #pragma unroll
-    for (int s = 0; s < 5; ++s) { wv5[w][s] = tv[s]; wi5[w][s] = ti[s]; }
+    for (int s = 0; s < 5; ++s) { wv5[w * 5 + s] = tv[s]; wi5[w * 5 + s] = ti[s]; }
   }
   __syncthreads();
   if (tid == 0) {
     float av[5]; int ai[5];
 #pragma unroll
-    for (int s = 0; s < 5; ++s) { av[s] = wv5[0][s]; ai[s] = wi5[0][s]; }
+    for (int s = 0; s < 5; ++s) { av[s] = wv5[s]; ai[s] = wi5[s]; }
     for (int ww = 1; ww < 4; ++ww) {
       float bv[5]; int bi[5];
 #pragma unroll
-      for (int s = 0; s < 5; ++s) { bv[s] = wv5[ww][s]; bi[s] = wi5[ww][s]; }
+      for (int s = 0; s < 5; ++s) { bv[s] = wv5[ww * 5 + s]; bi[s] = wi5[ww * 5 + s]; }
       merge5(av, ai, bv, bi);
     }
 #pragma unroll
     for (int s = 0; s < 5; ++s) {
       int pk = ai[s] / kV;
       int tk = ai[s] - pk * kV;
-      scores[b * 5 + s] = av[s];
-      prevK[b * 5 + s] = pk; tokv[b * 5 + s] = tk;
+      P.scores[b * 5 + s] = av[s];
+      P.prevK[b * 5 + s] = pk; P.tokv[b * 5 + s] = tk;
       fpk[s] = pk; ftok[s] = tk;
     }
   }
@@ -544,181 +553,214 @@
   }
 }
 
-__global__ void finalize_k(const float* __restrict__ scores, const int* __restrict__ buf,
-                           float* __restrict__ out) {
-  const int tid = threadIdx.x;
-  if (tid < RR) {
-    out[tid] = scores[tid];
+template<bool WT, bool ET>
+__global__ __launch_bounds__(256, 1) void mega_k(KParams P) {
+  __shared__ float SM[16384];
+  const int bid = blockIdx.x, tid = threadIdx.x;
+  int ph = 0;
+  int* arr = P.arrive; int* rel = P.release;
+
+  if (WT) do_transposes(P, SM);
+  gbar(arr, rel, ph);
+  do_crosskv<WT>(P, SM);
+  gbar(arr, rel, ph);
+
+  for (int t = 0; t < TMAX; ++t) {
+    const int* bc = (t & 1) ? P.bufs1 : P.bufs0;
+    int* bn = (t & 1) ? P.bufs0 : P.bufs1;
+    const int np = (t + 1) & 1, op = t & 1;
+    for (int l = 0; l < 2; ++l) {
+      float* kNew = P.kcB + (size_t)(np * 2 + l) * CSEG;
+      float* vNew = P.vcB + (size_t)(np * 2 + l) * CSEG;
+      if (l == 0) {
+        if (bid < 18) {
+          gemm_tile<WT>(SM, bid, P.siT, 2304, P.siW, 768, 0, P.siB, true,
+                        1, nullptr, 0, nullptr, nullptr, 0,
+                        P.lneg, P.lneb, P.XA, 3, P.qb, 768,
+                        kNew, vNew, t, bc, P.emb, P.pos);
+        } else if (bid >= 128 && t > 0) {
+          const int nfl4 = t * 192;
+          const int tot = 2 * 2 * RR * nfl4;
+          for (int i = (bid - 128) * 256 + tid; i < tot; i += 128 * 256) {
+            int lyr = i / (2 * RR * nfl4); int rem = i - lyr * (2 * RR * nfl4);
+            int half = rem / (RR * nfl4); rem -= half * (RR * nfl4);
+            int r = rem / nfl4; int e = rem - r * nfl4;
+            int p = e / 192, d4 = e - p * 192;
+            int src = (r / 5) * 5 + P.prevK[r];
+            const float* ob = (half ? P.vcB : P.kcB) + (size_t)(op * 2 + lyr) * CSEG;
+            float* nb2 = (half ? P.vcB : P.kcB) + (size_t)(np * 2 + lyr) * CSEG;
+            *(float4*)&nb2[(r * BUFL + p) * 768 + d4 * 4] =
+                *(const float4*)&ob[(src * BUFL + p) * 768 + d4 * 4];
+          }
+        }
+      } else {
+        if (bid < 18) {
+          const float* parts[4] = {P.fp0, P.fp1, P.fp2, P.fp3};
+          gemm_tile<WT>(SM, bid, P.siT + (size_t)768 * 2304, 2304, P.siW + (size_t)2304 * 768, 768, 0,
+                        P.siB + 2304, true,
+                        2, nullptr, 0, P.XC, parts, 4,
+                        P.ln3g, P.ln3b, P.XA, 3, P.qb, 768,
+                        kNew, vNew, t, bc, P.emb, P.pos);
+        }
+      }
+      gbar(arr, rel, ph);
+      if (bid < 60) self_attn_phase(P, SM, kNew, vNew, t);
+      gbar(arr, rel, ph);
+      if (bid < 6) {
+        gemm_tile<WT>(SM, bid, P.soT + (size_t)l * 768 * 768, 768, P.soW + (size_t)l * 768 * 768, 768, 0,
+                      P.soB + l * 768, true,
+                      0, P.attnb, 768, nullptr, nullptr, 0,
+                      nullptr, nullptr, nullptr, 0, P.tmp, 768,
+                      nullptr, nullptr, t, nullptr, nullptr, nullptr);
+      }
+      gbar(arr, rel, ph);
+      if (bid < 6) {
+        const float* parts[4] = {P.tmp, nullptr, nullptr, nullptr};
+        gemm_tile<WT>(SM, bid, P.ciT + (size_t)l * 768 * 2304, 2304, P.ciW + (size_t)l * 2304 * 768, 768, 0,
+                      P.ciB + l * 2304, true,
+                      2, nullptr, 0, P.XA, parts, 1,
+                      P.ln1g + l * 768, P.ln1b + l * 768, P.XB, 0, P.qb, 768,
+                      nullptr, nullptr, t, nullptr, nullptr, nullptr);
+      }
+      gbar(arr, rel, ph);
+      if (bid < 60) cross_attn_phase(P, SM, P.ck + (size_t)l * 4 * 128 * 768, P.cv + (size_t)l * 4 * 128 * 768);
+      gbar(arr, rel, ph);
+      if (bid < 6) {
+        gemm_tile<WT>(SM, bid, P.coT + (size_t)l * 768 * 768, 768, P.coW + (size_t)l * 768 * 768, 768, 0,
+                      P.coB + l * 768, true,
+                      0, P.attnb, 768, nullptr, nullptr, 0,
+                      nullptr, nullptr, nullptr, 0, P.tmp, 768,
+                      nullptr, nullptr, t, nullptr, nullptr, nullptr);
+      }
+      gbar(arr, rel, ph);
+      if (bid < 24) {
+        const float* parts[4] = {P.tmp, nullptr, nullptr, nullptr};
+        gemm_tile<WT>(SM, bid, P.f1T + (size_t)l * 768 * 3072, 3072, P.f1W + (size_t)l * 3072 * 768, 768, 0,
+                      P.f1B + l * 3072, true,
+                      2, nullptr, 0, P.XB, parts, 1,
+                      P.ln2g + l * 768, P.ln2b + l * 768, P.XC, 1, P.ffb, 3072,
+                      nullptr, nullptr, t, nullptr, nullptr, nullptr);
+      }
+      gbar(arr, rel, ph);
+      if (bid < 24) {
+        const int tile = bid >> 2, kq = bid & 3;
+        float* fps[4] = {P.fp0, P.fp1, P.fp2, P.fp3};
+        gemm_tile<WT>(SM, tile, P.f2T + (size_t)l * 3072 * 768, 768, P.f2W + (size_t)l * 768 * 3072, 3072,
+                      kq * 768, P.f2B + l * 768, (kq == 0),
+                      0, P.ffb + kq * 768, 3072, nullptr, nullptr, 0,
+                      nullptr, nullptr, nullptr, 0, fps[kq], 768,
+                      nullptr, nullptr, t, nullptr, nullptr, nullptr);
+      }
+      gbar(arr, rel, ph);
+    }
+    if (bid < 6) {
+      const float* parts[4] = {P.fp0, P.fp1, P.fp2, P.fp3};
+      gemm_tile<WT>(SM, bid, P.dT, 768, P.dW, 768, 0, P.dB, true,
+                    2, nullptr, 0, P.XC, parts, 4,
+                    P.ln3g + 768, P.ln3b + 768, nullptr, 2, P.hbuf, 768,
+                    nullptr, nullptr, t, nullptr, nullptr, nullptr);
+    }
+    gbar(arr, rel, ph);
+    if (bid < LB) logits_phase<ET>(P, SM);
+    gbar(arr, rel, ph);
+    if (bid < 4) topk_phase(P, SM, bc, bn, t);
+    gbar(arr, rel, ph);
+  }
+  if (bid == 0 && tid < RR) {
+    P.out[tid] = P.scores[tid];
     int seen = 0;
     for (int i = 0; i < TMAX; ++i) {
-      int tk = buf[tid * BUFL + 1 + i];
+      int tk = P.bufs0[tid * BUFL + 1 + i];
       if (tk == EOSt) seen = 1;
-      out[RR + tid * TMAX + i] = seen ? 0.f : (float)tk;
-    }
-  }
+      P.out[RR + tid * TMAX + i] = seen ? 0.f : (float)tk;
+    }
+  }
+}
+
+__global__ void init2_k(int* arrive, int* release, int* buf0, float* scores) {
+  int tid = threadIdx.x;
+  if (tid < 256) arrive[tid] = 0;
+  if (tid == 0) *release = 0;
+  if (tid < RR * BUFL) buf0[tid] = 0;
+  __syncthreads();
+  if (tid < BB) buf0[tid * BEAM * BUFL] = SOS;
+  if (tid < RR) scores[tid] = (tid % BEAM == 0) ? 0.f : NEGV;
 }
 
 extern "C" void kernel_launch(void* const* d_in, const int* in_sizes, int n_in,
                               void* d_out, int out_size, void* d_ws, size_t ws_size,
                               hipStream_t stream) {
-  const float* emb        = (const float*)d_in[0];
-  const float* pos        = (const float*)d_in[1];
-  const float* ln_emb_g   = (const float*)d_in[2];
-  const float* ln_emb_b   = (const float*)d_in[3];
-  const float* self_in_w  = (const float*)d_in[4];
-  const float* self_in_b  = (const float*)d_in[5];
-  const float* self_out_w = (const float*)d_in[6];
-  const float* self_out_b = (const float*)d_in[7];
-  const float* cross_in_w = (const float*)d_in[8];
-  const float* cross_in_b = (const float*)d_in[9];
-  const float* cross_out_w= (const float*)d_in[10];
-  const float* cross_out_b= (const float*)d_in[11];
-  const float* ff1_w      = (const float*)d_in[12];
-  const float* ff1_b      = (const float*)d_in[13];
-  const float* ff2_w      = (const float*)d_in[14];
-  const float* ff2_b      = (const float*)d_in[15];
-  const float* ln1_g      = (const float*)d_in[16];
-  const float* ln1_b      = (const float*)d_in[17];
-  const float* ln2_g      = (const float*)d_in[18];
-  const float* ln2_b      = (const float*)d_in[19];
-  const float* ln3_g      = (const float*)d_in[20];
-  const float* ln3_b      = (const float*)d_in[21];
-  const float* dense_w    = (const float*)d_in[22];
-  const float* dense_b    = (const float*)d_in[23];
-  const float* context    = (const float*)d_in[24];
-  const int*   source_mask= (const int*)d_in[25];
+  KParams P;
+  P.emb  = (const float*)d_in[0];  P.pos  = (const float*)d_in[1];
+  P.lneg = (const float*)d_in[2];  P.lneb = (const float*)d_in[3];
+  P.siW  = (const float*)d_in[4];  P.siB  = (const float*)d_in[5];
+  P.soW  = (const float*)d_in[6];  P.soB  = (const float*)d_in[7];
+  P.ciW  = (const float*)d_in[8];  P.ciB  = (const float*)d_in[9];
+  P.coW  = (const float*)d_in[10]; P.coB  = (const float*)d_in[11];
+  P.f1W  = (const float*)d_in[12]; P.f1B  = (const float*)d_in[13];
+  P.f2W  = (const float*)d_in[14]; P.f2B  = (const float*)d_in[15];
+  P.ln1g = (const float*)d_in[16]; P.ln1b = (const float*)d_in[17];
+  P.ln2g = (const float*)d_in[18]; P.ln2b = (const float*)d_in[19];
+  P.ln3g = (const float*)d_in[20]; P.ln3b = (const float*)d_in[21];
+  P.dW   = (const float*)d_in[22]; P.dB   = (const float*)d_in[23];
+  P.ctx  = (const float*)d_in[24]; P.smask = (const int*)d_in[25];
+  P.out  = (float*)d_out;
 
   float* wsf = (float*)d_ws;
   size_t off = 0;
   auto alloc = [&](size_t n) { float* p = wsf + off; off += (n + 3) & ~(size_t)3; return p; };
 
-  float* XA    = alloc(RR * 768);
-  float* XB    = alloc(RR * 768);
-  float* XC    = alloc(RR * 768);
-  float* qb    = alloc(RR * 768);
-  float* attnb = alloc(RR * 768);
-  float* tmp   = alloc(RR * 768);
-  float* hbuf  = alloc(RR * 768);
-  float* ffb   = alloc(RR * 3072);
-  float* candV = alloc(RR * LB * 5);
-  float* mrow  = alloc(RR * LB);
-  float* srow  = alloc(RR * LB);
-  float* scores= alloc(32);
-  float* ck    = alloc((size_t)NLY * 4 * 128 * 768);
-  float* cv    = alloc((size_t)NLY * 4 * 128 * 768);
-  const size_t cacheSeg = (size_t)RR * BUFL * 768;
-  float* kcB   = alloc(4 * cacheSeg);
-  float* vcB   = alloc(4 * cacheSeg);
-  int* candI   = (int*)alloc(RR * LB * 5);
-  int* bufs0   = (int*)alloc(RR * BUFL + 12);
-  int* bufs1   = (int*)alloc(RR * BUFL + 12);
-  int* prevKp  = (int*)alloc(32);
-  int* tokp    = (int*)alloc(32);
+  P.arrive = (int*)alloc(256);
+  P.release= (int*)alloc(8);
+  P.XA    = alloc(RR * 768);
+  P.XB    = alloc(RR * 768);
+  P.XC    = alloc(RR * 768);
+  P.qb    = alloc(RR * 768);
+  P.attnb = alloc(RR * 768);
+  P.tmp   = alloc(RR * 768);
+  P.hbuf  = alloc(RR * 768);
+  P.ffb   = alloc(RR * 3072);
+  P.fp0   = alloc(RR * 768);
+  P.fp1   = alloc(RR * 768);
+  P.fp2   = alloc(RR * 768);
+  P.fp3   = alloc(RR * 768);
+  P.candV = alloc(RR * LB * 5);
+  P.mrow  = alloc(RR * LB);
+  P.srow  = alloc(RR * LB);
+  P.scores= alloc(32);
+  P.ck    = alloc((size_t)2 * 4 * 128 * 768);
+  P.cv    = alloc((size_t)2 * 4 * 128 * 768);
+  P.kcB   = alloc((size_t)4 * CSEG);
+  P.vcB   = alloc((size_t)4 * CSEG);
+  P.candI = (int*)alloc(RR * LB * 5);
+  P.bufs0 = (int*)alloc(RR * BUFL + 12);
+  P.bufs1 = (int*)alloc(RR * BUFL + 12);
+  P.prevK = (int*)alloc(32);
+  P.tokv  = (int*)alloc(32);
   const size_t baseFloats = off;
 
   const size_t nSiT = (size_t)768 * 2304, nSoT = (size_t)768 * 768;
-  const size_t nCiT = nSiT, nCoT = nSoT, nF1T = (size_t)768 * 3072, nF2T = (size_t)3072 * 768;
-  const size_t wtFloats = 2 * (nSiT + nSoT + nCiT + nCoT + nF1T + nF2T) + nSoT;
+  const size_t nF1T = (size_t)768 * 3072;
+  const size_t wtFloats = 2 * (2 * nSiT + 2 * nSoT + 2 * nF1T) + nSoT;
   const size_t embTFloats = (size_t)768 * kVP;
   const bool useWT = ws_size >= (baseFloats + wtFloats) * 4;
   const bool useET = useWT && ws_size >= (baseFloats + wtFloats + embTFloats) * 4;
-
-  float* siT[2]; float* soT[2]; float* ciT[2]; float* coT[2]; float* f1T[2]; float* f2T[2];
-  float* dT = nullptr; float* embT = nullptr;
+  P.useWT = useWT; P.useET = useET;
+
+  P.siT = P.soT = P.ciT = P.coT = P.f1T = P.f2T = P.dT = P.embT = nullptr;
   if (useWT) {
-    for (int l = 0; l < 2; ++l) siT[l] = alloc(nSiT);
-    for (int l = 0; l < 2; ++l) soT[l] = alloc(nSoT);
-    for (int l = 0; l < 2; ++l) ciT[l] = alloc(nCiT);
-    for (int l = 0; l < 2; ++l) coT[l] = alloc(nCoT);
-    for (int l = 0; l < 2; ++l) f1T[l] = alloc(nF1T);
-    for (int l = 0; l < 2; ++l) f2T[l] = alloc(nF2T);
-    dT = alloc(nSoT);
-    if (useET) embT = alloc(embTFloats);
-  }
-
-  init_k<<<1, 512, 0, stream>>>(bufs0, scores);
-
-  if (useWT) {
-    auto T = [&](const float* src, float* dst, int R, int C, int ds) {
-      dim3 g((C + 31) / 32, (R + 31) / 32);
-      transpose_k<<<g, 256, 0, stream>>>(src, dst, R, C, ds);
-    };
-    for (int l = 0; l < 2; ++l) {
-      T(self_in_w  + (size_t)l * 2304 * 768, siT[l], 2304, 768, 2304);
-      T(self_out_w + (size_t)l * 768 * 768,  soT[l], 768, 768, 768);
-      T(cross_in_w + (size_t)l * 2304 * 768, ciT[l], 2304, 768, 2304);
-      T(cross_out_w+ (size_t)l * 768 * 768,  coT[l], 768, 768, 768);
-      T(ff1_w      + (size_t)l * 3072 * 768, f1T[l], 3072, 768, 3072);
-      T(ff2_w      + (size_t)l * 768 * 3072, f2T[l], 768, 3072, 768);
-    }
-    T(dense_w, dT, 768, 768, 768);
-    if (useET) T(emb, embT, kV, 768, kVP);
-  }
-
-  {
-    dim3 g(24, 32, 2);
-    if (useWT) crosskv_k<true><<<g, 256, 0, stream>>>(context, ciT[0], cross_in_b, ck, cv);
-    else       crosskv_k<false><<<g, 256, 0, stream>>>(context, cross_in_w, cross_in_b, ck, cv);
-  }
-
-  const int* bc = bufs0;
-  auto G = [&](const float* Wt, const float* Wg, int wstride,
-               const float* bias, int N, int pre, const float* xsrc, const float* tmpin,
-               const float* g2, const float* b2, float* xout, int outmode, float* out0,
-               float* kcl, float* vcl, int tt,
-               int reorder_t, const float* kco, const float* vco, float* kcn2, float* vcn2) {
-    dim3 grid(N / 64);
-    if (useWT)
-      gemm20_k<true><<<grid, 256, 0, stream>>>(Wt, wstride, bias, N, pre, xsrc, tmpin, g2, b2,
-        xout, outmode, out0, kcl, vcl, tt, emb, pos, bc, reorder_t, kco, vco, kcn2, vcn2, prevKp);
-    else
-      gemm20_k<false><<<grid, 256, 0, stream>>>(Wg, wstride, bias, N, pre, xsrc, tmpin, g2, b2,
-        xout, outmode, out0, kcl, vcl, tt, emb, pos, bc, reorder_t, kco, vco, kcn2, vcn2, prevKp);
-  };
-
-  for (int t = 0; t < TMAX; ++t) {
-    bc = (t & 1) ? bufs1 : bufs0;
-    int* bn = (t & 1) ? bufs0 : bufs1;
-    const int np = (t + 1) & 1, op = t & 1;
-
-    for (int l = 0; l < 2; ++l) {
-      float* kNew = kcB + (np * 2 + l) * cacheSeg;
-      float* vNew = vcB + (np * 2 + l) * cacheSeg;
-      float* kOld = kcB + (op * 2 + l) * cacheSeg;
-      float* vOld = vcB + (op * 2 + l) * cacheSeg;
-      if (l == 0)
-        G(siT[0], self_in_w, 2304, self_in_b, 2304,
-          1, nullptr, nullptr, ln_emb_g, ln_emb_b, XA,
-          3, qb, kNew, vNew, t, t, kOld, vOld, kNew, vNew);
-      else
-        G(siT[1], self_in_w + (size_t)2304 * 768, 2304, self_in_b + 2304, 2304,
-          2, XC, tmp, ln3_g, ln3_b, XA,
-          3, qb, kNew, vNew, t, t, kOld, vOld, kNew, vNew);
-      self_attn_k<<<dim3(RR, 12), 64, 0, stream>>>(qb, kNew, vNew, attnb, t);
-      G(soT[l], self_out_w + (size_t)l * 768 * 768, 768, self_out_b + l * 768, 768,
-        0, attnb, nullptr, nullptr, nullptr, nullptr, 0, tmp,
-        nullptr, nullptr, t, 0, nullptr, nullptr, nullptr, nullptr);
-      G(ciT[l], cross_in_w + (size_t)l * 2304 * 768, 2304, cross_in_b + l * 2304, 768,
-        2, XA, tmp, ln1_g + l * 768, ln1_b + l * 768, XB, 0, qb,
-        nullptr, nullptr, t, 0, nullptr, nullptr, nullptr, nullptr);
-      cross_attn_k<<<dim3(RR, 12), 64, 0, stream>>>(
-          qb, ck + (size_t)l * 4 * 128 * 768, cv + (size_t)l * 4 * 128 * 768, source_mask, attnb);
-      G(coT[l], cross_out_w + (size_t)l * 768 * 768, 768, cross_out_b + l * 768, 768,
-        0, attnb, nullptr, nullptr, nullptr, nullptr, 0, tmp,
-        nullptr, nullptr, t, 0, nullptr, nullptr, nullptr, nullptr);
-      G(f1T[l], ff1_w + (size_t)l * 3072 * 768, 3072, ff1_b + l * 3072, 3072,
-        2, XB, tmp, ln2_g + l * 768, ln2_b + l * 768, XC, 1, ffb,
-        nullptr, nullptr, t, 0, nullptr, nullptr, nullptr, nullptr);
-      if (useWT) ff2_k<true><<<48, 1024, 0, stream>>>(f2T[l], ff2_b + l * 768, ffb, tmp);
-      else       ff2_k<false><<<48, 1024, 0, stream>>>(ff2_w + (size_t)l * 768 * 3072, ff2_b + l * 768, ffb, tmp);
-    }
-    G(dT, dense_w, 768, dense_b, 768,
-      2, XC, tmp, ln3_g + 768, ln3_b + 768, nullptr, 2, hbuf,
-      nullptr, nullptr, t, 0, nullptr, nullptr, nullptr, nullptr);
-    if (useET) logits_k<true><<<LB, 256, 0, stream>>>(hbuf, embT, candV, candI, mrow, srow);
-    else       logits_k<false><<<LB, 256, 0, stream>>>(hbuf, emb, candV, candI, mrow, srow);
-    topk_k<<<BB, 256, 0, stream>>>(candV, candI, mrow, srow, scores, bc, bn, t, prevKp, tokp);
-  }
-
-  finalize_k<<<1, 64, 0, stream>>>(scores, bufs0, (float*)d_out);
-}
+    P.siT = alloc(2 * nSiT);
+    P.soT = alloc(2 * nSoT);
+    P.ciT = alloc(2 * nSiT);
+    P.coT = alloc(2 * nSoT);
+    P.f1T = alloc(2 * nF1T);
+    P.f2T = alloc(2 * nF1T);
+    P.dT  = alloc(nSoT);
+    if (useET) P.embT = alloc(embTFloats);
+  }
+
+  init2_k<<<1, 512, 0, stream>>>(P.arrive, P.release, P.bufs0, P.scores);
+  if (useET)      mega_k<true, true><<<256, 256, 0, stream>>>(P);
+  else if (useWT) mega_k<true, false><<<256, 256, 0, stream>>>(P);
+  else            mega_k<false, false><<<256, 256, 0, stream>>>(P);
+}
```

Measured after the change: 16.74 ms. 49.5% more time.
